# Kernel tuning notes

Hardware: AMD Instinct MI355X
Metric: run time of the kernel (lower is better)

## Reference

```python
import jax, jax.numpy as jnp
import numpy as np

N, E, D0, D1, H = 20000, 640000, 64, 32, 64


def setup_inputs() -> dict:
    key = jax.random.key(0)
    ks = jax.random.split(key, 16)
    s = 0.1
    return {
        'feat0e': jax.random.normal(ks[0], (N, D0), jnp.float32),
        'feat1o': jax.random.normal(ks[1], (N, D1, 3), jnp.float32),
        'edge_attr': jax.random.normal(ks[2], (E, H), jnp.float32),
        'pos': jax.random.normal(ks[3], (N, 3), jnp.float32),
        'edge_index': jax.random.randint(ks[4], (2, E), 0, N, jnp.int64),
        # edge_net: FullyConnectedNet([H]*3 -> [H]) with silu
        'W1': jax.random.normal(ks[5], (H, H), jnp.float32) * s,
        'b1': jnp.zeros((H,), jnp.float32),
        'W2': jax.random.normal(ks[6], (H, H), jnp.float32) * s,
        'b2': jnp.zeros((H,), jnp.float32),
        'W3': jax.random.normal(ks[7], (H, H), jnp.float32) * s,
        'b3': jnp.zeros((H,), jnp.float32),
        # tensor-product path weights (internal weights, not shared)
        'w_ss': jax.random.normal(ks[8], (D0, H, D0), jnp.float32) * s,     # 0e x 0e -> 0e
        'w_vv': jax.random.normal(ks[9], (D1, D0), jnp.float32) * s,        # 1o . 1o -> 0e
        'w_sv': jax.random.normal(ks[10], (D0, D1), jnp.float32) * s,       # 0e x 1o -> 1o
        'w_vs': jax.random.normal(ks[11], (D1, H, D1), jnp.float32) * s,    # 1o x 0e -> 1o
        'w_cross': jax.random.normal(ks[12], (D1, D1), jnp.float32) * s,    # 1o x 1o -> 1o (cross)
        # gate: scalars -> per-vector-channel gates
        'Wg': jax.random.normal(ks[13], (D0, D1), jnp.float32) * s,
        'bg': jnp.zeros((D1,), jnp.float32),
    }


def reference(feat0e, feat1o, edge_attr, pos, edge_index,
              W1, b1, W2, b2, W3, b3,
              w_ss, w_vv, w_sv, w_vs, w_cross, Wg, bg):
    src, dst = edge_index[0], edge_index[1]

    # edge MLP (silu)
    h = jax.nn.silu(edge_attr @ W1 + b1)
    h = jax.nn.silu(h @ W2 + b2)
    edge_scalar = h @ W3 + b3                      # [E, H]

    rel_pos = pos[dst] - pos[src]                  # [E, 3]
    s_src = feat0e[src]                            # [E, D0]
    v_src = feat1o[src]                            # [E, D1, 3]

    # equivariant tensor product per edge
    dot_vv = jnp.sum(v_src * rel_pos[:, None, :], axis=-1)          # [E, D1]
    msg0e = (jnp.einsum('ep,eh,pho->eo', s_src, edge_scalar, w_ss)
             + dot_vv @ w_vv)                                        # [E, D0]
    cross_vv = jnp.cross(v_src, rel_pos[:, None, :])                 # [E, D1, 3]
    msg1o = (jnp.einsum('ep,pc,ex->ecx', s_src, w_sv, rel_pos)
             + jnp.einsum('edx,eh,dhc->ecx', v_src, edge_scalar, w_vs)
             + jnp.einsum('edx,dc->ecx', cross_vv, w_cross))          # [E, D1, 3]

    # scatter_mean over destination nodes
    counts = jax.ops.segment_sum(jnp.ones((E,), msg0e.dtype), dst, num_segments=N)
    denom = jnp.maximum(counts, 1.0)
    aggr0e = jax.ops.segment_sum(msg0e, dst, num_segments=N) / denom[:, None]
    aggr1o = jax.ops.segment_sum(msg1o, dst, num_segments=N) / denom[:, None, None]

    # gate + residual
    out0e = jax.nn.silu(aggr0e) + feat0e                              # [N, D0]
    gates = jax.nn.silu(aggr0e @ Wg + bg)                             # [N, D1]
    out1o = aggr1o * gates[:, :, None] + feat1o                       # [N, D1, 3]

    # concat flattened outputs into one array [N, D0 + 3*D1]
    return jnp.concatenate([out0e, out1o.reshape(N, D1 * 3)], axis=-1)
```

## Files before the change

### kernel.cpp

```cpp
#include <hip/hip_runtime.h>


#define NN 20000
#define EE 640000
#define D0 64
#define D1 32
#define HH 64
#define EPMAX 940032

typedef _Float16 half8 __attribute__((ext_vector_type(8)));
typedef _Float16 half4 __attribute__((ext_vector_type(4)));
typedef float f32x4 __attribute__((ext_vector_type(4)));

__device__ __forceinline__ float silu_f(float x) { return x / (1.0f + __expf(-x)); }
__device__ __forceinline__ _Float16 u2h(unsigned short u) {
    union { unsigned short u; _Float16 h; } c; c.u = u; return c.h;
}
__device__ __forceinline__ unsigned short h2u(_Float16 h) {
    union { unsigned short u; _Float16 h; } c; c.h = h; return c.u;
}
__device__ __forceinline__ half8 pack8(float4 a, float4 b) {
    half8 h;
    h[0]=(_Float16)a.x; h[1]=(_Float16)a.y; h[2]=(_Float16)a.z; h[3]=(_Float16)a.w;
    h[4]=(_Float16)b.x; h[5]=(_Float16)b.y; h[6]=(_Float16)b.z; h[7]=(_Float16)b.w;
    return h;
}

#define OFF_HIST  0ull
#define OFF_RS    81920ull
#define OFF_CUR   163840ull
#define OFF_FLAG  245760ull
#define OFF_SRCA  262144ull
#define OFF_DSTA  2822144ull
#define OFF_PE    5382144ull
#define OFF_WSS   7942144ull
#define OFF_WVS2  8466432ull
#define OFF_WVV   8597504ull
#define OFF_WSV   8601600ull
#define OFF_WX    8605696ull
#define OFF_WMLP  8607744ull
#define OFF_MSG   8632320ull
#define WS_R4_NEED 131512320ull
#define OFF_WSSG  131512320ull
#define OFF_OUTD  132036608ull
#define OFF_PSP   132118528ull
#define OFF_CURS  132200448ull
#define OFF_DSTP  132282368ull
#define OFF_PEP   136042496ull
#define OFF_PDP   139802624ull
#define OFF_G     143562752ull
#define NEED_S(npp) (OFF_G + (unsigned long long)(npp) * 8192ull)

__global__ void detect_idx_kernel(const int* __restrict__ eidx, int* __restrict__ flag) {
    int odd_nz = 0, even_nz = 0;
    for (int k = 0; k < 64; ++k) {
        if (eidx[2 * k + 1] != 0) odd_nz = 1;
        if (eidx[2 * k] != 0) even_nz = 1;
    }
    *flag = (!odd_nz && even_nz) ? 1 : 0;
}

__device__ __forceinline__ void load_sd(const int* eidx, const int* flag, int e,
                                        int& s_, int& d_) {
    if (*flag) { s_ = (int)((const long long*)eidx)[e]; d_ = (int)((const long long*)eidx)[EE + e]; }
    else       { s_ = eidx[e];                          d_ = eidx[EE + e]; }
}

__global__ __launch_bounds__(256) void hist_kernel(
    const int* __restrict__ eidx, const int* __restrict__ flag, int* __restrict__ hist)
{
    const int e = blockIdx.x * 256 + threadIdx.x;
    int s_, d_; load_sd(eidx, flag, e, s_, d_);
    atomicAdd(hist + d_, 1);
}

__global__ __launch_bounds__(256) void hist2_kernel(
    const int* __restrict__ eidx, const int* __restrict__ flag,
    int* __restrict__ hist, int* __restrict__ outd)
{
    const int e = blockIdx.x * 256 + threadIdx.x;
    int s_, d_; load_sd(eidx, flag, e, s_, d_);
    atomicAdd(hist + d_, 1);
    atomicAdd(outd + s_, 1);
}

__global__ __launch_bounds__(1024) void scan_kernel(
    const int* __restrict__ hist, int* __restrict__ rs, int* __restrict__ cur)
{
    __shared__ int part[1024];
    const int t = threadIdx.x;
    const int base = t * 20;
    int loc[20];
    int tot = 0;
#pragma unroll
    for (int k = 0; k < 20; ++k) {
        int n = base + k;
        int h = (n < NN) ? hist[n] : 0;
        loc[k] = tot; tot += h;
    }
    part[t] = tot;
    __syncthreads();
    for (int off = 1; off < 1024; off <<= 1) {
        int v = (t >= off) ? part[t - off] : 0;
        __syncthreads();
        part[t] += v;
        __syncthreads();
    }
    int excl = part[t] - tot;
#pragma unroll
    for (int k = 0; k < 20; ++k) {
        int n = base + k;
        if (n < NN) { rs[n] = excl + loc[k]; cur[n] = excl + loc[k]; }
    }
    if (t == 1023) rs[NN] = part[1023];
}

__global__ __launch_bounds__(1024) void scanP_kernel(
    const int* __restrict__ outd, int* __restrict__ psP, int* __restrict__ curS)
{
    __shared__ int part[1024];
    const int t = threadIdx.x;
    const int base = t * 20;
    int loc[20];
    int tot = 0;
#pragma unroll
    for (int k = 0; k < 20; ++k) {
        int n = base + k;
        int p = (n < NN) ? ((outd[n] + 15) & ~15) : 0;
        loc[k] = tot; tot += p;
    }
    part[t] = tot;
    __syncthreads();
    for (int off = 1; off < 1024; off <<= 1) {
        int v = (t >= off) ? part[t - off] : 0;
        __syncthreads();
        part[t] += v;
        __syncthreads();
    }
    int excl = part[t] - tot;
#pragma unroll
    for (int k = 0; k < 20; ++k) {
        int n = base + k;
        if (n < NN) { psP[n] = excl + loc[k]; curS[n] = excl + loc[k]; }
    }
}

__global__ __launch_bounds__(256) void scat_both_kernel(
    const int* __restrict__ eidx, const int* __restrict__ flag,
    int* __restrict__ curS, int* __restrict__ cur,
    int* __restrict__ dstP, int* __restrict__ peP, int* __restrict__ pdP,
    int* __restrict__ srca, int* __restrict__ dsta, int* __restrict__ pe)
{
    const int e = blockIdx.x * 256 + threadIdx.x;
    int s_, d_; load_sd(eidx, flag, e, s_, d_);
    int posS = atomicAdd(curS + s_, 1);
    int posD = atomicAdd(cur + d_, 1);
    dstP[posS] = d_; peP[posS] = e; pdP[posS] = posD;
    srca[posD] = s_; dsta[posD] = d_; pe[posD] = e;
}

__global__ __launch_bounds__(256) void scatter_r4_kernel(
    const int* __restrict__ eidx, const int* __restrict__ flag,
    int* __restrict__ cur, int* __restrict__ srca, int* __restrict__ dsta,
    int* __restrict__ pe)
{
    const int e = blockIdx.x * 256 + threadIdx.x;
    int s_, d_; load_sd(eidx, flag, e, s_, d_);
    int pos = atomicAdd(cur + d_, 1);
    srca[pos] = s_; dsta[pos] = d_; pe[pos] = e;
}

__global__ __launch_bounds__(256) void prep_kernel(
    const float* __restrict__ wss, const float* __restrict__ wvv,
    const float* __restrict__ wsv, const float* __restrict__ wvs,
    const float* __restrict__ wx,
    const float* __restrict__ W1, const float* __restrict__ W2,
    const float* __restrict__ W3, char* __restrict__ ws, int maxid)
{
    int id = blockIdx.x * 256 + threadIdx.x;
    if (id >= maxid) return;
    int l = id & 63;
    int l4 = l >> 4, l16 = l & 15;
    half8 o;
    _Float16* dst;
    if (id < 32768) {
        int p = id >> 9; int frag = (id >> 6) & 7;
        int kf = frag >> 2, nf = frag & 3;
#pragma unroll
        for (int j = 0; j < 8; j++) {
            int h = kf * 32 + l4 * 8 + j, oo = nf * 16 + l16;
            o[j] = (_Float16)wss[((size_t)p * 64 + h) * 64 + oo];
        }
        dst = (_Float16*)(ws + OFF_WSS) + (size_t)id * 8;
    } else if (id < 40960) {
        int i = id - 32768;
        int f = i >> 6;
        int chunk = f >> 3, kf = (f >> 2) & 1, nfl = f & 3;
#pragma unroll
        for (int j = 0; j < 8; j++) {
            int h = kf * 32 + l4 * 8 + j;
            int col = chunk * 64 + nfl * 16 + l16;
            int d = col >> 5, c = col & 31;
            o[j] = (_Float16)wvs[((size_t)d * 64 + h) * 32 + c];
        }
        dst = (_Float16*)(ws + OFF_WVS2) + (size_t)i * 8;
    } else if (id < 41216) {
        int i = id - 40960; int nf = i >> 6;
#pragma unroll
        for (int j = 0; j < 8; j++) {
            int d = l4 * 8 + j, oo = nf * 16 + l16;
            o[j] = (_Float16)wvv[d * 64 + oo];
        }
        dst = (_Float16*)(ws + OFF_WVV) + (size_t)i * 8;
    } else if (id < 41472) {
        int i = id - 41216; int frag = i >> 6;
        int kf = frag >> 1, nf = frag & 1;
#pragma unroll
        for (int j = 0; j < 8; j++) {
            int p = kf * 32 + l4 * 8 + j, c = nf * 16 + l16;
            o[j] = (_Float16)wsv[p * 32 + c];
        }
        dst = (_Float16*)(ws + OFF_WSV) + (size_t)i * 8;
    } else if (id < 41600) {
        int i = id - 41472; int nf = i >> 6;
#pragma unroll
        for (int j = 0; j < 8; j++) {
            int d = l4 * 8 + j, c = nf * 16 + l16;
            o[j] = (_Float16)wx[d * 32 + c];
        }
        dst = (_Float16*)(ws + OFF_WX) + (size_t)i * 8;
    } else if (id < 43136) {
        int i = id - 41600; int f = i >> 6;
        int layer = f >> 3, kf = (f >> 2) & 1, nf = f & 3;
        const float* W = layer == 0 ? W1 : (layer == 1 ? W2 : W3);
#pragma unroll
        for (int j = 0; j < 8; j++) {
            int r = kf * 32 + l4 * 8 + j, cc = nf * 16 + l16;
            o[j] = (_Float16)W[r * 64 + cc];
        }
        dst = (_Float16*)(ws + OFF_WMLP) + (size_t)i * 8;
    } else {
        int i = id - 43136;
        int f = i >> 6;
        int q = f >> 3, kfp = (f >> 2) & 1, nfp = f & 3;
#pragma unroll
        for (int j = 0; j < 8; j++) {
            int p = kfp * 32 + l4 * 8 + j;
            int cc = q * 64 + nfp * 16 + l16;
            int jc = cc & 7, lc = (cc >> 3) & 63, fi = cc >> 9;
            int kfc = fi >> 2, nfc = fi & 3;
            int h = kfc * 32 + (lc >> 4) * 8 + jc;
            int oo = nfc * 16 + (lc & 15);
            o[j] = (_Float16)wss[((size_t)p * 64 + h) * 64 + oo];
        }
        dst = (_Float16*)(ws + OFF_WSSG) + (size_t)i * 8;
    }
    *(half8*)dst = o;
}

__global__ __launch_bounds__(256, 2) void gG_kernel(
    const float* __restrict__ feat0e, const char* __restrict__ wsp,
    int lo, int hi, _Float16* __restrict__ G)
{
    const int tid = threadIdx.x, w = tid >> 6, lane = tid & 63;
    const int l4 = lane >> 4, l16 = lane & 15;
    const int n0 = lo + blockIdx.x * 64 + w * 16;
    if (n0 >= hi) return;

    half8 af[2];
    {
        int n = n0 + l16; if (n >= NN) n = NN - 1;
        const float* sp = feat0e + (size_t)n * 64 + l4 * 8;
        af[0] = pack8(*(const float4*)sp, *(const float4*)(sp + 4));
        af[1] = pack8(*(const float4*)(sp + 32), *(const float4*)(sp + 36));
    }
    const half8* wg = (const half8*)(wsp + OFF_WSSG);
    for (int q = 0; q < 64; ++q) {
        f32x4 acc[4];
#pragma unroll
        for (int nf = 0; nf < 4; nf++) acc[nf] = (f32x4){0.f,0.f,0.f,0.f};
#pragma unroll
        for (int kf = 0; kf < 2; kf++)
#pragma unroll
            for (int nf = 0; nf < 4; nf++)
                acc[nf] = __builtin_amdgcn_mfma_f32_16x16x32_f16(
                    af[kf], wg[(q * 8 + kf * 4 + nf) * 64 + lane], acc[nf], 0, 0, 0);
#pragma unroll
        for (int nf = 0; nf < 4; nf++)
#pragma unroll
            for (int reg = 0; reg < 4; reg++) {
                int n = n0 + l4 * 4 + reg;
                if (n < hi && n < NN)
                    G[(size_t)(n - lo) * 4096 + q * 64 + nf * 16 + l16] =
                        (_Float16)acc[nf][reg];
            }
    }
}

__device__ __forceinline__ void mlp_wave(
    const float* __restrict__ edge_attr,
    const float* __restrict__ b1, const float* __restrict__ b2,
    const float* __restrict__ b3,
    const char* __restrict__ wsp,
    const int* __restrict__ pel_w,
    unsigned short* __restrict__ xch,
    int lane, half8 esf[4][2])
{
    const int l4 = lane >> 4, l16 = lane & 15;
    const half8* wm = (const half8*)(wsp + OFF_WMLP);

    float bias[3][4];
#pragma unroll
    for (int nf = 0; nf < 4; nf++) {
        bias[0][nf] = b1[nf * 16 + l16];
        bias[1][nf] = b2[nf * 16 + l16];
        bias[2][nf] = b3[nf * 16 + l16];
    }

    half8 af[4][2];
#pragma unroll
    for (int mf = 0; mf < 4; mf++) {
        int e = pel_w[mf * 16 + l16];
        const float* p = edge_attr + (size_t)e * 64 + l4 * 8;
#pragma unroll
        for (int kf = 0; kf < 2; kf++)
            af[mf][kf] = pack8(*(const float4*)(p + kf * 32),
                               *(const float4*)(p + kf * 32 + 4));
    }

#pragma unroll
    for (int layer = 0; layer < 3; ++layer) {
        f32x4 acc[4][4];
#pragma unroll
        for (int mf = 0; mf < 4; mf++)
#pragma unroll
            for (int nf = 0; nf < 4; nf++) acc[mf][nf] = (f32x4){0.f,0.f,0.f,0.f};
#pragma unroll
        for (int kf = 0; kf < 2; kf++)
#pragma unroll
            for (int mf = 0; mf < 4; mf++)
#pragma unroll
                for (int nf = 0; nf < 4; nf++)
                    acc[mf][nf] = __builtin_amdgcn_mfma_f32_16x16x32_f16(
                        af[mf][kf], wm[(layer * 8 + kf * 4 + nf) * 64 + lane],
                        acc[mf][nf], 0, 0, 0);
#pragma unroll
        for (int mf = 0; mf < 4; mf++)
#pragma unroll
            for (int nf = 0; nf < 4; nf++)
#pragma unroll
                for (int reg = 0; reg < 4; reg++) {
                    int row = mf * 16 + l4 * 4 + reg;
                    int col = nf * 16 + l16;
                    float v = acc[mf][nf][reg] + bias[layer][nf];
                    if (layer < 2) v = silu_f(v);
                    xch[row * 64 + (col ^ ((row & 7) << 3))] = h2u((_Float16)v);
                }
        if (layer < 2) {
#pragma unroll
            for (int mf = 0; mf < 4; mf++)
#pragma unroll
                for (int kf = 0; kf < 2; kf++) {
                    int row = mf * 16 + l16;
                    int cs = kf * 32 + l4 * 8;
                    af[mf][kf] = *(const half8*)&xch[row * 64 + (cs ^ ((row & 7) << 3))];
                }
        }
    }
#pragma unroll
    for (int mf = 0; mf < 4; mf++)
#pragma unroll
        for (int kf = 0; kf < 2; kf++) {
            int row = mf * 16 + l16;
            int cs = kf * 32 + l4 * 8;
            esf[mf][kf] = *(const half8*)&xch[row * 64 + (cs ^ ((row & 7) << 3))];
        }
}

__global__ __launch_bounds__(256, 3) void msg0e_node_kernel(
    const float* __restrict__ feat1o,
    const float* __restrict__ edge_attr,
    const float* __restrict__ pos,
    const float* __restrict__ b1, const float* __restrict__ b2,
    const float* __restrict__ b3,
    const char* __restrict__ wsp,
    const _Float16* __restrict__ G,
    int lo, int hi,
    _Float16* __restrict__ msg0)
{
    __shared__ half8 wml[1536];
    __shared__ __align__(16) unsigned short xch[4][1024];

    const int tid = threadIdx.x, w = tid >> 6, lane = tid & 63;
    const int l4 = lane >> 4, l16 = lane & 15;

    {
        const half8* wm = (const half8*)(wsp + OFF_WMLP);
        for (int f = tid; f < 1536; f += 256) wml[f] = wm[f];
    }
    __syncthreads();

    const int n = lo + blockIdx.x * 4 + w;
    if (n >= hi) return;
    const int deg = ((const int*)(wsp + OFF_OUTD))[n];
    if (deg == 0) return;
    const int base = ((const int*)(wsp + OFF_PSP))[n];
    const int* dstP = (const int*)(wsp + OFF_DSTP);
    const int* peP  = (const int*)(wsp + OFF_PEP);
    const int* pdP  = (const int*)(wsp + OFF_PDP);

    const float pn0 = pos[n * 3 + 0], pn1 = pos[n * 3 + 1], pn2 = pos[n * 3 + 2];
    half8 Gr[8];
    {
        const half8* gn = (const half8*)G + (size_t)(n - lo) * 512;
#pragma unroll
        for (int f = 0; f < 8; f++) Gr[f] = gn[f * 64 + lane];
    }
    half8 wvvf[4];
    {
        const half8* wvvp = (const half8*)(wsp + OFF_WVV);
#pragma unroll
        for (int nf = 0; nf < 4; nf++) wvvf[nf] = wvvp[nf * 64 + lane];
    }
    float vx[8], vy[8], vz[8];
#pragma unroll
    for (int j = 0; j < 8; j++) {
        int d = l4 * 8 + j;
        vx[j] = feat1o[(size_t)n * 96 + d * 3 + 0];
        vy[j] = feat1o[(size_t)n * 96 + d * 3 + 1];
        vz[j] = feat1o[(size_t)n * 96 + d * 3 + 2];
    }
    float bias[3][4];
#pragma unroll
    for (int nf = 0; nf < 4; nf++) {
        bias[0][nf] = b1[nf * 16 + l16];
        bias[1][nf] = b2[nf * 16 + l16];
        bias[2][nf] = b3[nf * 16 + l16];
    }

    unsigned short* x = xch[w];
    const int ntile = (deg + 15) >> 4;
    const int sw16 = (l16 & 7) << 3;

    for (int t = 0; t < ntile; ++t) {
        const int r0 = t * 16;
        int rowc = r0 + l16; if (rowc > deg - 1) rowc = deg - 1;
        const int pe = peP[base + rowc];
        const int dd = dstP[base + rowc];
        const float rel0 = pos[dd * 3 + 0] - pn0;
        const float rel1 = pos[dd * 3 + 1] - pn1;
        const float rel2 = pos[dd * 3 + 2] - pn2;

        half8 af[2];
        {
            const float* ap = edge_attr + (size_t)pe * 64 + l4 * 8;
            af[0] = pack8(*(const float4*)ap, *(const float4*)(ap + 4));
            af[1] = pack8(*(const float4*)(ap + 32), *(const float4*)(ap + 36));
        }
#pragma unroll
        for (int layer = 0; layer < 3; ++layer) {
            f32x4 acc[4];
#pragma unroll
            for (int nf = 0; nf < 4; nf++) acc[nf] = (f32x4){0.f,0.f,0.f,0.f};
#pragma unroll
            for (int kf = 0; kf < 2; kf++)
#pragma unroll
                for (int nf = 0; nf < 4; nf++)
                    acc[nf] = __builtin_amdgcn_mfma_f32_16x16x32_f16(
                        af[kf], wml[(layer * 8 + kf * 4 + nf) * 64 + lane],
                        acc[nf], 0, 0, 0);
#pragma unroll
            for (int nf = 0; nf < 4; nf++)
#pragma unroll
                for (int reg = 0; reg < 4; reg++) {
                    int row = l4 * 4 + reg;
                    int col = nf * 16 + l16;
                    float v = acc[nf][reg] + bias[layer][nf];
                    if (layer < 2) v = silu_f(v);
                    x[row * 64 + (col ^ ((row & 7) << 3))] = h2u((_Float16)v);
                }
            if (layer < 2) {
#pragma unroll
                for (int kf = 0; kf < 2; kf++)
                    af[kf] = *(const half8*)&x[l16 * 64 + ((kf * 32 + l4 * 8) ^ sw16)];
            }
        }
        half8 esf[2];
#pragma unroll
        for (int kf = 0; kf < 2; kf++)
            esf[kf] = *(const half8*)&x[l16 * 64 + ((kf * 32 + l4 * 8) ^ sw16)];

        f32x4 acc[4];
#pragma unroll
        for (int nf = 0; nf < 4; nf++) acc[nf] = (f32x4){0.f,0.f,0.f,0.f};
#pragma unroll
        for (int kf = 0; kf < 2; kf++)
#pragma unroll
            for (int nf = 0; nf < 4; nf++)
                acc[nf] = __builtin_amdgcn_mfma_f32_16x16x32_f16(
                    esf[kf], Gr[kf * 4 + nf], acc[nf], 0, 0, 0);
        half8 dvf;
#pragma unroll
        for (int j = 0; j < 8; j++)
            dvf[j] = (_Float16)(vx[j] * rel0 + vy[j] * rel1 + vz[j] * rel2);
#pragma unroll
        for (int nf = 0; nf < 4; nf++)
            acc[nf] = __builtin_amdgcn_mfma_f32_16x16x32_f16(
                dvf, wvvf[nf], acc[nf], 0, 0, 0);

#pragma unroll
        for (int nf = 0; nf < 4; nf++)
#pragma unroll
            for (int reg = 0; reg < 4; reg++) {
                int row = l4 * 4 + reg;
                int col = nf * 16 + l16;
                x[row * 64 + (col ^ ((row & 7) << 3))] = h2u((_Float16)acc[nf][reg]);
            }
#pragma unroll
        for (int i = 0; i < 2; i++) {
            int row16 = i * 8 + (lane >> 3);
            if (r0 + row16 < deg) {
                int rowD = pdP[base + r0 + row16];
                int c8 = lane & 7;
                half8 v = *(const half8*)&x[row16 * 64 + ((c8 * 8) ^ ((row16 & 7) << 3))];
                *(half8*)(msg0 + (size_t)rowD * 64 + c8 * 8) = v;
            }
        }
    }
}

__global__ __launch_bounds__(256, 2) void msg0e_r4_kernel(
    const float* __restrict__ feat0e,
    const float* __restrict__ feat1o,
    const float* __restrict__ edge_attr,
    const float* __restrict__ pos,
    const float* __restrict__ b1, const float* __restrict__ b2,
    const float* __restrict__ b3,
    const char* __restrict__ wsp,
    _Float16* __restrict__ msg0)
{
    __shared__ unsigned short st[4][4096];
    __shared__ unsigned short wf[16384];
    __shared__ float rell[4][64][3];
    __shared__ int   srcl[4][64];
    __shared__ int   pel[4][64];

    const int tid = threadIdx.x, w = tid >> 6, lane = tid & 63;
    const int l4 = lane >> 4, l16 = lane & 15;
    const long i0 = (long)blockIdx.x * 256 + w * 64;

    {
        long p = i0 + lane;
        int s_ = ((const int*)(wsp + OFF_SRCA))[p];
        int d_ = ((const int*)(wsp + OFF_DSTA))[p];
        pel[w][lane] = ((const int*)(wsp + OFF_PE))[p];
        srcl[w][lane] = s_;
        rell[w][lane][0] = pos[d_ * 3 + 0] - pos[s_ * 3 + 0];
        rell[w][lane][1] = pos[d_ * 3 + 1] - pos[s_ * 3 + 1];
        rell[w][lane][2] = pos[d_ * 3 + 2] - pos[s_ * 3 + 2];
    }
    __syncthreads();

    half8 esf[4][2];
    mlp_wave(edge_attr, b1, b2, b3, wsp, pel[w], st[w], lane, esf);
    __syncthreads();

#pragma unroll
    for (int r4 = 0; r4 < 4; r4++) {
        int row = r4 * 16 + (lane >> 2);
        int ch = lane & 3;
        const float* sp = feat0e + (size_t)srcl[w][row] * 64 + ch * 16;
        half8 h0 = pack8(*(const float4*)(sp + 0), *(const float4*)(sp + 4));
        half8 h1 = pack8(*(const float4*)(sp + 8), *(const float4*)(sp + 12));
        int r7 = row & 7;
        *(half8*)&st[w][row * 64 + (((ch * 2) ^ r7) * 8)]     = h0;
        *(half8*)&st[w][row * 64 + (((ch * 2 + 1) ^ r7) * 8)] = h1;
    }
    __syncthreads();

    f32x4 acc[4][4];
#pragma unroll
    for (int mf = 0; mf < 4; mf++)
#pragma unroll
        for (int nf = 0; nf < 4; nf++) acc[mf][nf] = (f32x4){0.f, 0.f, 0.f, 0.f};

    const half8* wss_g = (const half8*)(wsp + OFF_WSS);
    half8* wfh = (half8*)wf;
    for (int pc = 0; pc < 16; ++pc) {
        __syncthreads();
#pragma unroll
        for (int q = 0; q < 8; q++)
            wfh[q * 256 + tid] = wss_g[pc * 2048 + q * 256 + tid];
        __syncthreads();
#pragma unroll
        for (int pl = 0; pl < 4; ++pl) {
            const int p = pc * 4 + pl;
            _Float16 sv[4];
#pragma unroll
            for (int mf = 0; mf < 4; mf++) {
                int row = mf * 16 + l16;
                sv[mf] = u2h(st[w][row * 64 + (((p >> 3) ^ (row & 7)) * 8) + (p & 7)]);
            }
#pragma unroll
            for (int kf = 0; kf < 2; kf++) {
                half8 bf[4];
#pragma unroll
                for (int nf = 0; nf < 4; nf++)
                    bf[nf] = wfh[(pl * 8 + kf * 4 + nf) * 64 + lane];
#pragma unroll
                for (int mf = 0; mf < 4; mf++) {
                    half8 a = esf[mf][kf] * sv[mf];
#pragma unroll
                    for (int nf = 0; nf < 4; nf++)
                        acc[mf][nf] = __builtin_amdgcn_mfma_f32_16x16x32_f16(a, bf[nf], acc[mf][nf], 0, 0, 0);
                }
            }
        }
    }

    half8 dvf[4];
#pragma unroll
    for (int mf = 0; mf < 4; mf++) {
        int row = mf * 16 + l16;
        int se = srcl[w][row];
        float r0 = rell[w][row][0], r1 = rell[w][row][1], r2 = rell[w][row][2];
        const float* vp = feat1o + (size_t)se * 96 + l4 * 24;
        float4 A = *(const float4*)(vp + 0),  B = *(const float4*)(vp + 4);
        float4 C = *(const float4*)(vp + 8),  D = *(const float4*)(vp + 12);
        float4 E = *(const float4*)(vp + 16), F = *(const float4*)(vp + 20);
        dvf[mf][0] = (_Float16)(A.x * r0 + A.y * r1 + A.z * r2);
        dvf[mf][1] = (_Float16)(A.w * r0 + B.x * r1 + B.y * r2);
        dvf[mf][2] = (_Float16)(B.z * r0 + B.w * r1 + C.x * r2);
        dvf[mf][3] = (_Float16)(C.y * r0 + C.z * r1 + C.w * r2);
        dvf[mf][4] = (_Float16)(D.x * r0 + D.y * r1 + D.z * r2);
        dvf[mf][5] = (_Float16)(D.w * r0 + E.x * r1 + E.y * r2);
        dvf[mf][6] = (_Float16)(E.z * r0 + E.w * r1 + F.x * r2);
        dvf[mf][7] = (_Float16)(F.y * r0 + F.z * r1 + F.w * r2);
    }
    const half8* wvvp = (const half8*)(wsp + OFF_WVV);
#pragma unroll
    for (int nf = 0; nf < 4; nf++) {
        half8 bvv = wvvp[nf * 64 + lane];
#pragma unroll
        for (int mf = 0; mf < 4; mf++)
            acc[mf][nf] = __builtin_amdgcn_mfma_f32_16x16x32_f16(dvf[mf], bvv, acc[mf][nf], 0, 0, 0);
    }

#pragma unroll
    for (int mf = 0; mf < 4; mf++)
#pragma unroll
        for (int nf = 0; nf < 4; nf++)
#pragma unroll
            for (int reg = 0; reg < 4; reg++) {
                int row = mf * 16 + l4 * 4 + reg;
                int col = nf * 16 + l16;
                st[w][row * 64 + (col ^ ((row & 7) << 3))] = h2u((_Float16)acc[mf][nf][reg]);
            }
#pragma unroll
    for (int t = 0; t < 8; t++) {
        int row = t * 8 + (lane >> 3);
        int c8 = lane & 7;
        half8 v = *(const half8*)&st[w][row * 64 + ((c8 * 8) ^ ((row & 7) << 3))];
        *(half8*)(msg0 + (size_t)(i0 + row) * 64 + c8 * 8) = v;
    }
}

__global__ __launch_bounds__(256, 2) void msg1o_kernel(
    const float* __restrict__ feat0e,
    const float* __restrict__ feat1o,
    const float* __restrict__ edge_attr,
    const float* __restrict__ pos,
    const float* __restrict__ b1, const float* __restrict__ b2,
    const float* __restrict__ b3,
    const char* __restrict__ wsp,
    _Float16* __restrict__ msg1)
{
    __shared__ unsigned short vt[4][6144];
    __shared__ float rell[4][64][3];
    __shared__ int srcl[4][64];
    __shared__ int pel[4][64];

    const int tid = threadIdx.x, w = tid >> 6, lane = tid & 63;
    const int l4 = lane >> 4, l16 = lane & 15;
    const long i0 = (long)blockIdx.x * 256 + w * 64;

    {
        long p = i0 + lane;
        int s_ = ((const int*)(wsp + OFF_SRCA))[p];
        int d_ = ((const int*)(wsp + OFF_DSTA))[p];
        pel[w][lane] = ((const int*)(wsp + OFF_PE))[p];
        srcl[w][lane] = s_;
        rell[w][lane][0] = pos[d_ * 3 + 0] - pos[s_ * 3 + 0];
        rell[w][lane][1] = pos[d_ * 3 + 1] - pos[s_ * 3 + 1];
        rell[w][lane][2] = pos[d_ * 3 + 2] - pos[s_ * 3 + 2];
    }
    __syncthreads();

    half8 esf[4][2];
    mlp_wave(edge_attr, b1, b2, b3, wsp, pel[w], vt[w], lane, esf);
    __syncthreads();

    {
        const float* vp = feat1o + (size_t)srcl[w][lane] * 96;
#pragma unroll
        for (int q = 0; q < 24; q++) {
            float4 f = *(const float4*)(vp + q * 4);
            vt[w][(q * 4 + 0) * 64 + lane] = h2u((_Float16)f.x);
            vt[w][(q * 4 + 1) * 64 + lane] = h2u((_Float16)f.y);
            vt[w][(q * 4 + 2) * 64 + lane] = h2u((_Float16)f.z);
            vt[w][(q * 4 + 3) * 64 + lane] = h2u((_Float16)f.w);
        }
    }
    __syncthreads();

    const half8* wvs2p = (const half8*)(wsp + OFF_WVS2);
    const half8* wsvp  = (const half8*)(wsp + OFF_WSV);
    const half8* wxp   = (const half8*)(wsp + OFF_WX);

    f32x4 acc1[4][3][2];
#pragma unroll
    for (int g = 0; g < 4; g++)
#pragma unroll
        for (int x = 0; x < 3; x++)
#pragma unroll
            for (int ch = 0; ch < 2; ch++) acc1[g][x][ch] = (f32x4){0.f,0.f,0.f,0.f};

#pragma unroll 2
    for (int ck = 0; ck < 16; ++ck) {
        half8 bf[2][4];
#pragma unroll
        for (int kf = 0; kf < 2; kf++)
#pragma unroll
            for (int nfl = 0; nfl < 4; nfl++)
                bf[kf][nfl] = wvs2p[(ck * 8 + kf * 4 + nfl) * 64 + lane];
#pragma unroll
        for (int g = 0; g < 4; g++) {
            f32x4 tacc[4];
#pragma unroll
            for (int nfl = 0; nfl < 4; nfl++) tacc[nfl] = (f32x4){0.f,0.f,0.f,0.f};
#pragma unroll
            for (int kf = 0; kf < 2; kf++)
#pragma unroll
                for (int nfl = 0; nfl < 4; nfl++)
                    tacc[nfl] = __builtin_amdgcn_mfma_f32_16x16x32_f16(
                        esf[g][kf], bf[kf][nfl], tacc[nfl], 0, 0, 0);
#pragma unroll
            for (int dl = 0; dl < 2; dl++) {
                int d = ck * 2 + dl;
#pragma unroll
                for (int x = 0; x < 3; x++) {
                    half4 hv = *(const half4*)&vt[w][(d * 3 + x) * 64 + g * 16 + l4 * 4];
                    f32x4 vf = __builtin_convertvector(hv, f32x4);
                    acc1[g][x][0] += vf * tacc[dl * 2 + 0];
                    acc1[g][x][1] += vf * tacc[dl * 2 + 1];
                }
            }
        }
    }

    {
        half8 bsv[2][2];
#pragma unroll
        for (int kf = 0; kf < 2; kf++)
#pragma unroll
            for (int nf = 0; nf < 2; nf++)
                bsv[kf][nf] = wsvp[(size_t)(kf * 2 + nf) * 64 + lane];
#pragma unroll
        for (int g = 0; g < 4; g++) {
            int erow = g * 16 + l16;
            const float* sp = feat0e + (size_t)srcl[w][erow] * 64 + l4 * 8;
            half8 sf[2];
#pragma unroll
            for (int kf = 0; kf < 2; kf++)
                sf[kf] = pack8(*(const float4*)(sp + kf * 32),
                               *(const float4*)(sp + kf * 32 + 4));
#pragma unroll
            for (int x = 0; x < 3; x++) {
                _Float16 rl = (_Float16)rell[w][erow][x];
#pragma unroll
                for (int kf = 0; kf < 2; kf++) {
                    half8 a = sf[kf] * rl;
#pragma unroll
                    for (int nf = 0; nf < 2; nf++)
                        acc1[g][x][nf] = __builtin_amdgcn_mfma_f32_16x16x32_f16(
                            a, bsv[kf][nf], acc1[g][x][nf], 0, 0, 0);
                }
            }
        }
    }

    {
        half8 bx[2];
        bx[0] = wxp[lane];
        bx[1] = wxp[64 + lane];
#pragma unroll
        for (int g = 0; g < 4; g++) {
            f32x4 cx[3][2];
#pragma unroll
            for (int xp = 0; xp < 3; xp++) {
                half8 av;
#pragma unroll
                for (int j = 0; j < 8; j++)
                    av[j] = u2h(vt[w][((l4 * 8 + j) * 3 + xp) * 64 + g * 16 + l16]);
#pragma unroll
                for (int nf = 0; nf < 2; nf++)
                    cx[xp][nf] = __builtin_amdgcn_mfma_f32_16x16x32_f16(
                        av, bx[nf], (f32x4){0.f,0.f,0.f,0.f}, 0, 0, 0);
            }
            f32x4 r[3];
#pragma unroll
            for (int x = 0; x < 3; x++)
#pragma unroll
                for (int reg = 0; reg < 4; reg++)
                    r[x][reg] = rell[w][g * 16 + l4 * 4 + reg][x];
#pragma unroll
            for (int x = 0; x < 3; x++) {
                const int x1 = (x + 1) % 3, x2 = (x + 2) % 3;
#pragma unroll
                for (int ch = 0; ch < 2; ch++)
                    acc1[g][x][ch] += r[x2] * cx[x1][ch] - r[x1] * cx[x2][ch];
            }
        }
    }

    __syncthreads();
#pragma unroll
    for (int g = 0; g < 4; g++)
#pragma unroll
        for (int reg = 0; reg < 4; reg++) {
            int row = g * 16 + l4 * 4 + reg;
            int sw = (row & 3) << 3;
#pragma unroll
            for (int x = 0; x < 3; x++)
#pragma unroll
                for (int ch = 0; ch < 2; ch++) {
                    int c32 = ch * 16 + l16;
                    vt[w][row * 96 + x * 32 + (c32 ^ sw)] = h2u((_Float16)acc1[g][x][ch][reg]);
                }
        }
#pragma unroll
    for (int tt = 0; tt < 12; tt++) {
        int x = tt >> 2, rem = (tt & 3) * 8;
        int col = x * 32 + (rem ^ ((lane & 3) << 3));
        half8 v = *(const half8*)&vt[w][lane * 96 + col];
        *(half8*)(msg1 + (size_t)(i0 + lane) * 96 + tt * 8) = v;
    }
}

__global__ __launch_bounds__(256) void gather0_kernel(
    const float* __restrict__ feat0e,
    const float* __restrict__ Wg, const float* __restrict__ bg,
    const char* __restrict__ wsp, const _Float16* __restrict__ msg0,
    float* __restrict__ out)
{
    __shared__ float Wgl[2048];
    __shared__ float ag[4][64];
    const int tid = threadIdx.x, w = tid >> 6, lane = tid & 63;
    for (int t = tid; t < 2048; t += 256) Wgl[t] = Wg[t];

    const int n = blockIdx.x * 4 + w;
    const int* rs = (const int*)(wsp + OFF_RS);
    const int i0 = rs[n], i1 = rs[n + 1];
    const int r8 = lane >> 3, c8 = lane & 7;

    float a[8];
#pragma unroll
    for (int j = 0; j < 8; j++) a[j] = 0.f;
    for (int i = i0 + r8; i < i1; i += 8) {
        half8 m = *(const half8*)(msg0 + (size_t)i * 64 + c8 * 8);
#pragma unroll
        for (int j = 0; j < 8; j++) a[j] += (float)m[j];
    }
#pragma unroll
    for (int s = 8; s < 64; s <<= 1)
#pragma unroll
        for (int j = 0; j < 8; j++) a[j] += __shfl_xor(a[j], s);
    if (r8 == 0)
#pragma unroll
        for (int j = 0; j < 8; j++) ag[w][c8 * 8 + j] = a[j];
    __syncthreads();

    const float inv = 1.0f / fmaxf((float)(i1 - i0), 1.0f);
    float av = ag[w][lane] * inv;
    out[(size_t)n * 160 + lane] = silu_f(av) + feat0e[(size_t)n * 64 + lane];

    if (lane < 32) {
        float gs = bg[lane];
#pragma unroll
        for (int p = 0; p < 64; ++p) gs = fmaf(ag[w][p] * inv, Wgl[p * 32 + lane], gs);
        out[(size_t)n * 160 + 64 + lane] = silu_f(gs);
    }
}

__global__ __launch_bounds__(256) void gather1_kernel(
    const float* __restrict__ feat1o,
    const char* __restrict__ wsp, const _Float16* __restrict__ msg1,
    float* __restrict__ out)
{
    __shared__ float ag1[4][96];
    __shared__ float gl[4][32];
    const int tid = threadIdx.x, w = tid >> 6, lane = tid & 63;
    const int n = blockIdx.x * 4 + w;
    const int* rs = (const int*)(wsp + OFF_RS);
    const int i0 = rs[n], i1 = rs[n + 1];

    if (lane < 32) gl[w][lane] = out[(size_t)n * 160 + 64 + lane];

    const int r4 = lane >> 4, c12 = lane & 15;
    float a[8];
#pragma unroll
    for (int j = 0; j < 8; j++) a[j] = 0.f;
    if (c12 < 12)
        for (int i = i0 + r4; i < i1; i += 4) {
            half8 m = *(const half8*)(msg1 + (size_t)i * 96 + c12 * 8);
#pragma unroll
            for (int j = 0; j < 8; j++) a[j] += (float)m[j];
        }
#pragma unroll
    for (int s = 16; s < 64; s <<= 1)
#pragma unroll
        for (int j = 0; j < 8; j++) a[j] += __shfl_xor(a[j], s);
    if (r4 == 0 && c12 < 12)
#pragma unroll
        for (int j = 0; j < 8; j++) ag1[w][c12 * 8 + j] = a[j];
    __syncthreads();

    const float inv = 1.0f / fmaxf((float)(i1 - i0), 1.0f);
#pragma unroll
    for (int t = 0; t < 2; t++) {
        int idx = t * 64 + lane;
        if (idx < 96) {
            int c = idx / 3, x = idx - 3 * c;
            float v = ag1[w][x * 32 + c] * inv * gl[w][c] + feat1o[(size_t)n * 96 + idx];
            out[(size_t)n * 160 + 64 + idx] = v;
        }
    }
}

extern "C" void kernel_launch(void* const* d_in, const int* in_sizes, int n_in,
                              void* d_out, int out_size, void* d_ws, size_t ws_size,
                              hipStream_t stream) {
    const float* feat0e    = (const float*)d_in[0];
    const float* feat1o    = (const float*)d_in[1];
    const float* edge_attr = (const float*)d_in[2];
    const float* pos       = (const float*)d_in[3];
    const int*   eidx      = (const int*)d_in[4];
    const float* W1 = (const float*)d_in[5];
    const float* b1 = (const float*)d_in[6];
    const float* W2 = (const float*)d_in[7];
    const float* b2 = (const float*)d_in[8];
    const float* W3 = (const float*)d_in[9];
    const float* b3 = (const float*)d_in[10];
    const float* wss    = (const float*)d_in[11];
    const float* wvv    = (const float*)d_in[12];
    const float* wsv    = (const float*)d_in[13];
    const float* wvs    = (const float*)d_in[14];
    const float* wcross = (const float*)d_in[15];
    const float* Wg = (const float*)d_in[16];
    const float* bg = (const float*)d_in[17];

    float* out = (float*)d_out;
    char*  ws  = (char*)d_ws;
    int* hist = (int*)(ws + OFF_HIST);
    int* rs   = (int*)(ws + OFF_RS);
    int* cur  = (int*)(ws + OFF_CUR);
    int* flag = (int*)(ws + OFF_FLAG);
    int* srca = (int*)(ws + OFF_SRCA);
    int* dsta = (int*)(ws + OFF_DSTA);
    int* pe   = (int*)(ws + OFF_PE);
    _Float16* msg = (_Float16*)(ws + OFF_MSG);

    detect_idx_kernel<<<1, 1, 0, stream>>>(eidx, flag);
    hipMemsetAsync(ws + OFF_HIST, 0, NN * sizeof(int), stream);

    int S = 0;
    if (ws_size >= NEED_S(20000)) S = 1;
    else if (ws_size >= NEED_S(10000)) S = 2;
    else if (ws_size >= NEED_S(5000))  S = 4;
    else if (ws_size >= NEED_S(2500))  S = 8;

    if (S > 0) {
        int* outd = (int*)(ws + OFF_OUTD);
        int* psP  = (int*)(ws + OFF_PSP);
        int* curS = (int*)(ws + OFF_CURS);
        int* dstP = (int*)(ws + OFF_DSTP);
        int* peP  = (int*)(ws + OFF_PEP);
        int* pdP  = (int*)(ws + OFF_PDP);
        _Float16* G = (_Float16*)(ws + OFF_G);

        hipMemsetAsync(ws + OFF_OUTD, 0, NN * sizeof(int), stream);

        hist2_kernel<<<EE / 256, 256, 0, stream>>>(eidx, flag, hist, outd);
        scan_kernel<<<1, 1024, 0, stream>>>(hist, rs, cur);
        scanP_kernel<<<1, 1024, 0, stream>>>(outd, psP, curS);
        scat_both_kernel<<<EE / 256, 256, 0, stream>>>(
            eidx, flag, curS, cur, dstP, peP, pdP, srca, dsta, pe);
        prep_kernel<<<(75904 + 255) / 256, 256, 0, stream>>>(
            wss, wvv, wsv, wvs, wcross, W1, W2, W3, ws, 75904);

        const int npp = (NN + S - 1) / S;
        for (int s = 0; s < S; ++s) {
            int lo = s * npp;
            int hi = lo + npp; if (hi > NN) hi = NN;
            gG_kernel<<<(hi - lo + 63) / 64, 256, 0, stream>>>(
                feat0e, (const char*)ws, lo, hi, G);
            msg0e_node_kernel<<<(hi - lo + 3) / 4, 256, 0, stream>>>(
                feat1o, edge_attr, pos, b1, b2, b3, (const char*)ws, G, lo, hi, msg);
        }
        gather0_kernel<<<NN / 4, 256, 0, stream>>>(
            feat0e, Wg, bg, (const char*)ws, msg, out);
        msg1o_kernel<<<EE / 256, 256, 0, stream>>>(
            feat0e, feat1o, edge_attr, pos, b1, b2, b3, (const char*)ws, msg);
        gather1_kernel<<<NN / 4, 256, 0, stream>>>(
            feat1o, (const char*)ws, msg, out);
    } else {
        hist_kernel<<<EE / 256, 256, 0, stream>>>(eidx, flag, hist);
        scan_kernel<<<1, 1024, 0, stream>>>(hist, rs, cur);
        scatter_r4_kernel<<<EE / 256, 256, 0, stream>>>(eidx, flag, cur, srca, dsta, pe);
        prep_kernel<<<(43136 + 255) / 256, 256, 0, stream>>>(
            wss, wvv, wsv, wvs, wcross, W1, W2, W3, ws, 43136);
        msg0e_r4_kernel<<<EE / 256, 256, 0, stream>>>(
            feat0e, feat1o, edge_attr, pos, b1, b2, b3, (const char*)ws, msg);
        gather0_kernel<<<NN / 4, 256, 0, stream>>>(
            feat0e, Wg, bg, (const char*)ws, msg, out);
        msg1o_kernel<<<EE / 256, 256, 0, stream>>>(
            feat0e, feat1o, edge_attr, pos, b1, b2, b3, (const char*)ws, msg);
        gather1_kernel<<<NN / 4, 256, 0, stream>>>(
            feat1o, (const char*)ws, msg, out);
    }
}
```

Baseline: 849.5 us.

## Precompute per-source-node tensor-product projections and fuse msg0e/msg1o into one node pass

Moves the per-edge tensor-product weight contractions to per-source-node precomputation. gG2 and gH build G/H tables from feat0e and feat1o against w_ss, w_vs, w_vv, w_sv and w_cross. A separate es_kernel computes the edge MLP once into a buffer, and a single msg01_node_kernel walks edges grouped by source to produce both msg0e and msg1o. This replaces the separate per-edge msg1o kernel and removes the fallback path. The aim is to remove redundant per-edge MFMA work and a second pass over edge_attr, at the cost of a much larger workspace footprint (GH per node plus ES/MSG buffers). If the workspace is too small the function now returns without computing anything.

```diff
diff --git a/kernel.cpp b/kernel.cpp
--- a/kernel.cpp
+++ b/kernel.cpp
@@ -3,13 +3,9 @@
 
 #define NN 20000
 #define EE 640000
-#define D0 64
-#define D1 32
-#define HH 64
 #define EPMAX 940032
 
 typedef _Float16 half8 __attribute__((ext_vector_type(8)));
-typedef _Float16 half4 __attribute__((ext_vector_type(4)));
 typedef float f32x4 __attribute__((ext_vector_type(4)));
 
 __device__ __forceinline__ float silu_f(float x) { return x / (1.0f + __expf(-x)); }
@@ -30,26 +26,24 @@
 #define OFF_RS    81920ull
 #define OFF_CUR   163840ull
 #define OFF_FLAG  245760ull
-#define OFF_SRCA  262144ull
-#define OFF_DSTA  2822144ull
-#define OFF_PE    5382144ull
-#define OFF_WSS   7942144ull
-#define OFF_WVS2  8466432ull
-#define OFF_WVV   8597504ull
-#define OFF_WSV   8601600ull
-#define OFF_WX    8605696ull
-#define OFF_WMLP  8607744ull
-#define OFF_MSG   8632320ull
-#define WS_R4_NEED 131512320ull
-#define OFF_WSSG  131512320ull
-#define OFF_OUTD  132036608ull
-#define OFF_PSP   132118528ull
-#define OFF_CURS  132200448ull
-#define OFF_DSTP  132282368ull
-#define OFF_PEP   136042496ull
-#define OFF_PDP   139802624ull
-#define OFF_G     143562752ull
-#define NEED_S(npp) (OFF_G + (unsigned long long)(npp) * 8192ull)
+#define F_OUTD    262144ull
+#define F_PSP     360448ull
+#define F_CURS    458752ull
+#define F_POSOF   557056ull
+#define F_AUX     3117056ull
+#define F_DSTP    23597056ull
+#define F_PDP     27357184ull
+#define F_WMLP    31117312ull
+#define F_WSV     31141888ull
+#define F_WX2     31145984ull
+#define F_WVV     31148032ull
+#define F_WSSG    31152128ull
+#define F_WVS3    31676416ull
+#define F_ES      31807488ull
+#define F_MSG0    152131584ull
+#define F_MSG1    234051584ull
+#define F_GH      356931584ull
+#define NEED_F(npp) (F_GH + (unsigned long long)(npp) * 20480ull)
 
 __global__ void detect_idx_kernel(const int* __restrict__ eidx, int* __restrict__ flag) {
     int odd_nz = 0, even_nz = 0;
@@ -64,14 +58,6 @@
                                         int& s_, int& d_) {
     if (*flag) { s_ = (int)((const long long*)eidx)[e]; d_ = (int)((const long long*)eidx)[EE + e]; }
     else       { s_ = eidx[e];                          d_ = eidx[EE + e]; }
-}
-
-__global__ __launch_bounds__(256) void hist_kernel(
-    const int* __restrict__ eidx, const int* __restrict__ flag, int* __restrict__ hist)
-{
-    const int e = blockIdx.x * 256 + threadIdx.x;
-    int s_, d_; load_sd(eidx, flag, e, s_, d_);
-    atomicAdd(hist + d_, 1);
 }
 
 __global__ __launch_bounds__(256) void hist2_kernel(
@@ -145,102 +131,33 @@
     }
 }
 
-__global__ __launch_bounds__(256) void scat_both_kernel(
+__global__ __launch_bounds__(256) void scat_src_kernel(
     const int* __restrict__ eidx, const int* __restrict__ flag,
     int* __restrict__ curS, int* __restrict__ cur,
-    int* __restrict__ dstP, int* __restrict__ peP, int* __restrict__ pdP,
-    int* __restrict__ srca, int* __restrict__ dsta, int* __restrict__ pe)
+    int* __restrict__ dstP, int* __restrict__ pdP, int* __restrict__ posof)
 {
     const int e = blockIdx.x * 256 + threadIdx.x;
     int s_, d_; load_sd(eidx, flag, e, s_, d_);
     int posS = atomicAdd(curS + s_, 1);
     int posD = atomicAdd(cur + d_, 1);
-    dstP[posS] = d_; peP[posS] = e; pdP[posS] = posD;
-    srca[posD] = s_; dsta[posD] = d_; pe[posD] = e;
-}
-
-__global__ __launch_bounds__(256) void scatter_r4_kernel(
-    const int* __restrict__ eidx, const int* __restrict__ flag,
-    int* __restrict__ cur, int* __restrict__ srca, int* __restrict__ dsta,
-    int* __restrict__ pe)
-{
-    const int e = blockIdx.x * 256 + threadIdx.x;
-    int s_, d_; load_sd(eidx, flag, e, s_, d_);
-    int pos = atomicAdd(cur + d_, 1);
-    srca[pos] = s_; dsta[pos] = d_; pe[pos] = e;
-}
-
-__global__ __launch_bounds__(256) void prep_kernel(
+    dstP[posS] = d_; pdP[posS] = posD; posof[e] = posS;
+}
+
+__global__ __launch_bounds__(256) void prep2_kernel(
     const float* __restrict__ wss, const float* __restrict__ wvv,
     const float* __restrict__ wsv, const float* __restrict__ wvs,
     const float* __restrict__ wx,
     const float* __restrict__ W1, const float* __restrict__ W2,
-    const float* __restrict__ W3, char* __restrict__ ws, int maxid)
+    const float* __restrict__ W3, char* __restrict__ ws)
 {
     int id = blockIdx.x * 256 + threadIdx.x;
-    if (id >= maxid) return;
+    if (id >= 43136) return;
     int l = id & 63;
     int l4 = l >> 4, l16 = l & 15;
     half8 o;
     _Float16* dst;
     if (id < 32768) {
-        int p = id >> 9; int frag = (id >> 6) & 7;
-        int kf = frag >> 2, nf = frag & 3;
-#pragma unroll
-        for (int j = 0; j < 8; j++) {
-            int h = kf * 32 + l4 * 8 + j, oo = nf * 16 + l16;
-            o[j] = (_Float16)wss[((size_t)p * 64 + h) * 64 + oo];
-        }
-        dst = (_Float16*)(ws + OFF_WSS) + (size_t)id * 8;
-    } else if (id < 40960) {
-        int i = id - 32768;
-        int f = i >> 6;
-        int chunk = f >> 3, kf = (f >> 2) & 1, nfl = f & 3;
-#pragma unroll
-        for (int j = 0; j < 8; j++) {
-            int h = kf * 32 + l4 * 8 + j;
-            int col = chunk * 64 + nfl * 16 + l16;
-            int d = col >> 5, c = col & 31;
-            o[j] = (_Float16)wvs[((size_t)d * 64 + h) * 32 + c];
-        }
-        dst = (_Float16*)(ws + OFF_WVS2) + (size_t)i * 8;
-    } else if (id < 41216) {
-        int i = id - 40960; int nf = i >> 6;
-#pragma unroll
-        for (int j = 0; j < 8; j++) {
-            int d = l4 * 8 + j, oo = nf * 16 + l16;
-            o[j] = (_Float16)wvv[d * 64 + oo];
-        }
-        dst = (_Float16*)(ws + OFF_WVV) + (size_t)i * 8;
-    } else if (id < 41472) {
-        int i = id - 41216; int frag = i >> 6;
-        int kf = frag >> 1, nf = frag & 1;
-#pragma unroll
-        for (int j = 0; j < 8; j++) {
-            int p = kf * 32 + l4 * 8 + j, c = nf * 16 + l16;
-            o[j] = (_Float16)wsv[p * 32 + c];
-        }
-        dst = (_Float16*)(ws + OFF_WSV) + (size_t)i * 8;
-    } else if (id < 41600) {
-        int i = id - 41472; int nf = i >> 6;
-#pragma unroll
-        for (int j = 0; j < 8; j++) {
-            int d = l4 * 8 + j, c = nf * 16 + l16;
-            o[j] = (_Float16)wx[d * 32 + c];
-        }
-        dst = (_Float16*)(ws + OFF_WX) + (size_t)i * 8;
-    } else if (id < 43136) {
-        int i = id - 41600; int f = i >> 6;
-        int layer = f >> 3, kf = (f >> 2) & 1, nf = f & 3;
-        const float* W = layer == 0 ? W1 : (layer == 1 ? W2 : W3);
-#pragma unroll
-        for (int j = 0; j < 8; j++) {
-            int r = kf * 32 + l4 * 8 + j, cc = nf * 16 + l16;
-            o[j] = (_Float16)W[r * 64 + cc];
-        }
-        dst = (_Float16*)(ws + OFF_WMLP) + (size_t)i * 8;
-    } else {
-        int i = id - 43136;
+        int i = id;
         int f = i >> 6;
         int q = f >> 3, kfp = (f >> 2) & 1, nfp = f & 3;
 #pragma unroll
@@ -253,14 +170,51 @@
             int oo = nfc * 16 + (lc & 15);
             o[j] = (_Float16)wss[((size_t)p * 64 + h) * 64 + oo];
         }
-        dst = (_Float16*)(ws + OFF_WSSG) + (size_t)i * 8;
+        dst = (_Float16*)(ws + F_WSSG) + (size_t)i * 8;
+    } else if (id < 40960) {
+        int i = id - 32768;
+        int f = i >> 6;
+        int col = f * 16 + l16;
+#pragma unroll
+        for (int j = 0; j < 8; j++) {
+            int d = l4 * 8 + j;
+            o[j] = (_Float16)wvs[((size_t)d * 64 + (col & 63)) * 32 + (col >> 6)];
+        }
+        dst = (_Float16*)(ws + F_WVS3) + (size_t)i * 8;
+    } else if (id < 42496) {
+        int i = id - 40960; int f = i >> 6;
+        int layer = f >> 3, kf = (f >> 2) & 1, nf = f & 3;
+        const float* W = layer == 0 ? W1 : (layer == 1 ? W2 : W3);
+#pragma unroll
+        for (int j = 0; j < 8; j++)
+            o[j] = (_Float16)W[(kf * 32 + l4 * 8 + j) * 64 + nf * 16 + l16];
+        dst = (_Float16*)(ws + F_WMLP) + (size_t)i * 8;
+    } else if (id < 42752) {
+        int i = id - 42496; int nf = i >> 6;
+#pragma unroll
+        for (int j = 0; j < 8; j++)
+            o[j] = (_Float16)wvv[(l4 * 8 + j) * 64 + nf * 16 + l16];
+        dst = (_Float16*)(ws + F_WVV) + (size_t)i * 8;
+    } else if (id < 43008) {
+        int i = id - 42752; int frag = i >> 6;
+        int kf = frag >> 1, nf = frag & 1;
+#pragma unroll
+        for (int j = 0; j < 8; j++)
+            o[j] = (_Float16)wsv[(kf * 32 + l4 * 8 + j) * 32 + nf * 16 + l16];
+        dst = (_Float16*)(ws + F_WSV) + (size_t)i * 8;
+    } else {
+        int i = id - 43008; int nf = i >> 6;
+#pragma unroll
+        for (int j = 0; j < 8; j++)
+            o[j] = (_Float16)wx[(l4 * 8 + j) * 32 + nf * 16 + l16];
+        dst = (_Float16*)(ws + F_WX2) + (size_t)i * 8;
     }
     *(half8*)dst = o;
 }
 
-__global__ __launch_bounds__(256, 2) void gG_kernel(
+__global__ __launch_bounds__(256, 2) void gG2_kernel(
     const float* __restrict__ feat0e, const char* __restrict__ wsp,
-    int lo, int hi, _Float16* __restrict__ G)
+    int lo, int hi, _Float16* __restrict__ GH, _Float16* __restrict__ aux)
 {
     const int tid = threadIdx.x, w = tid >> 6, lane = tid & 63;
     const int l4 = lane >> 4, l16 = lane & 15;
@@ -274,7 +228,7 @@
         af[0] = pack8(*(const float4*)sp, *(const float4*)(sp + 4));
         af[1] = pack8(*(const float4*)(sp + 32), *(const float4*)(sp + 36));
     }
-    const half8* wg = (const half8*)(wsp + OFF_WSSG);
+    const half8* wg = (const half8*)(wsp + F_WSSG);
     for (int q = 0; q < 64; ++q) {
         f32x4 acc[4];
 #pragma unroll
@@ -291,23 +245,113 @@
             for (int reg = 0; reg < 4; reg++) {
                 int n = n0 + l4 * 4 + reg;
                 if (n < hi && n < NN)
-                    G[(size_t)(n - lo) * 4096 + q * 64 + nf * 16 + l16] =
+                    GH[(size_t)(n - lo) * 10240 + q * 64 + nf * 16 + l16] =
                         (_Float16)acc[nf][reg];
             }
     }
-}
-
-__device__ __forceinline__ void mlp_wave(
+    {
+        const half8* wsvp = (const half8*)(wsp + F_WSV);
+        f32x4 accg[2];
+#pragma unroll
+        for (int nf = 0; nf < 2; nf++) accg[nf] = (f32x4){0.f,0.f,0.f,0.f};
+#pragma unroll
+        for (int kf = 0; kf < 2; kf++)
+#pragma unroll
+            for (int nf = 0; nf < 2; nf++)
+                accg[nf] = __builtin_amdgcn_mfma_f32_16x16x32_f16(
+                    af[kf], wsvp[(kf * 2 + nf) * 64 + lane], accg[nf], 0, 0, 0);
+#pragma unroll
+        for (int nf = 0; nf < 2; nf++)
+#pragma unroll
+            for (int reg = 0; reg < 4; reg++) {
+                int n = n0 + l4 * 4 + reg;
+                if (n < hi && n < NN)
+                    aux[(size_t)n * 512 + nf * 16 + l16] = (_Float16)accg[nf][reg];
+            }
+    }
+}
+
+__global__ __launch_bounds__(256, 2) void gH_kernel(
+    const float* __restrict__ feat1o, const char* __restrict__ wsp,
+    int lo, int hi, _Float16* __restrict__ GH, _Float16* __restrict__ aux)
+{
+    const int tid = threadIdx.x, w = tid >> 6, lane = tid & 63;
+    const int l4 = lane >> 4, l16 = lane & 15;
+    const int n0 = lo + blockIdx.x * 64 + w * 16;
+    if (n0 >= hi) return;
+
+    const half8* wvs3 = (const half8*)(wsp + F_WVS3);
+    const half8* wvvp = (const half8*)(wsp + F_WVV);
+    const half8* wx2  = (const half8*)(wsp + F_WX2);
+
+#pragma unroll 1
+    for (int x = 0; x < 3; ++x) {
+        half8 av;
+        {
+            int nn = n0 + l16; if (nn >= NN) nn = NN - 1;
+#pragma unroll
+            for (int j = 0; j < 8; j++)
+                av[j] = (_Float16)feat1o[(size_t)nn * 96 + (l4 * 8 + j) * 3 + x];
+        }
+#pragma unroll 4
+        for (int f = 0; f < 128; ++f) {
+            f32x4 acc = __builtin_amdgcn_mfma_f32_16x16x32_f16(
+                av, wvs3[f * 64 + lane], (f32x4){0.f,0.f,0.f,0.f}, 0, 0, 0);
+#pragma unroll
+            for (int reg = 0; reg < 4; reg++) {
+                int n = n0 + l4 * 4 + reg;
+                if (n < hi && n < NN)
+                    GH[(size_t)(n - lo) * 10240 + 4096 + x * 2048 + f * 16 + l16] =
+                        (_Float16)acc[reg];
+            }
+        }
+#pragma unroll
+        for (int nf = 0; nf < 4; ++nf) {
+            f32x4 acc = __builtin_amdgcn_mfma_f32_16x16x32_f16(
+                av, wvvp[nf * 64 + lane], (f32x4){0.f,0.f,0.f,0.f}, 0, 0, 0);
+#pragma unroll
+            for (int reg = 0; reg < 4; reg++) {
+                int n = n0 + l4 * 4 + reg;
+                if (n < hi && n < NN)
+                    aux[(size_t)n * 512 + 128 + x * 64 + nf * 16 + l16] =
+                        (_Float16)acc[reg];
+            }
+        }
+#pragma unroll
+        for (int nf = 0; nf < 2; ++nf) {
+            f32x4 acc = __builtin_amdgcn_mfma_f32_16x16x32_f16(
+                av, wx2[nf * 64 + lane], (f32x4){0.f,0.f,0.f,0.f}, 0, 0, 0);
+#pragma unroll
+            for (int reg = 0; reg < 4; reg++) {
+                int n = n0 + l4 * 4 + reg;
+                if (n < hi && n < NN)
+                    aux[(size_t)n * 512 + 32 + x * 32 + nf * 16 + l16] =
+                        (_Float16)acc[reg];
+            }
+        }
+    }
+}
+
+__global__ __launch_bounds__(256, 2) void es_kernel(
     const float* __restrict__ edge_attr,
     const float* __restrict__ b1, const float* __restrict__ b2,
     const float* __restrict__ b3,
-    const char* __restrict__ wsp,
-    const int* __restrict__ pel_w,
-    unsigned short* __restrict__ xch,
-    int lane, half8 esf[4][2])
-{
+    const char* __restrict__ wsp, const int* __restrict__ posof,
+    _Float16* __restrict__ es)
+{
+    __shared__ half8 wml[1536];
+    __shared__ __align__(16) unsigned short xch[4][1024];
+
+    const int tid = threadIdx.x, w = tid >> 6, lane = tid & 63;
     const int l4 = lane >> 4, l16 = lane & 15;
-    const half8* wm = (const half8*)(wsp + OFF_WMLP);
+
+    {
+        const half8* wm = (const half8*)(wsp + F_WMLP);
+        for (int f = tid; f < 1536; f += 256) wml[f] = wm[f];
+    }
+    __syncthreads();
+
+    const int e0 = blockIdx.x * 64 + w * 16;
 
     float bias[3][4];
 #pragma unroll
@@ -317,533 +361,203 @@
         bias[2][nf] = b3[nf * 16 + l16];
     }
 
-    half8 af[4][2];
-#pragma unroll
-    for (int mf = 0; mf < 4; mf++) {
-        int e = pel_w[mf * 16 + l16];
-        const float* p = edge_attr + (size_t)e * 64 + l4 * 8;
+    half8 af[2];
+    {
+        const float* ap = edge_attr + (size_t)(e0 + l16) * 64 + l4 * 8;
+        af[0] = pack8(*(const float4*)ap, *(const float4*)(ap + 4));
+        af[1] = pack8(*(const float4*)(ap + 32), *(const float4*)(ap + 36));
+    }
+
+    unsigned short* x = xch[w];
+    const int sw16 = (l16 & 7) << 3;
+
+#pragma unroll
+    for (int layer = 0; layer < 3; ++layer) {
+        f32x4 acc[4];
+#pragma unroll
+        for (int nf = 0; nf < 4; nf++) acc[nf] = (f32x4){0.f,0.f,0.f,0.f};
 #pragma unroll
         for (int kf = 0; kf < 2; kf++)
-            af[mf][kf] = pack8(*(const float4*)(p + kf * 32),
-                               *(const float4*)(p + kf * 32 + 4));
-    }
-
-#pragma unroll
-    for (int layer = 0; layer < 3; ++layer) {
-        f32x4 acc[4][4];
-#pragma unroll
-        for (int mf = 0; mf < 4; mf++)
-#pragma unroll
-            for (int nf = 0; nf < 4; nf++) acc[mf][nf] = (f32x4){0.f,0.f,0.f,0.f};
-#pragma unroll
-        for (int kf = 0; kf < 2; kf++)
-#pragma unroll
-            for (int mf = 0; mf < 4; mf++)
-#pragma unroll
-                for (int nf = 0; nf < 4; nf++)
-                    acc[mf][nf] = __builtin_amdgcn_mfma_f32_16x16x32_f16(
-                        af[mf][kf], wm[(layer * 8 + kf * 4 + nf) * 64 + lane],
-                        acc[mf][nf], 0, 0, 0);
-#pragma unroll
-        for (int mf = 0; mf < 4; mf++)
 #pragma unroll
             for (int nf = 0; nf < 4; nf++)
-#pragma unroll
-                for (int reg = 0; reg < 4; reg++) {
-                    int row = mf * 16 + l4 * 4 + reg;
-                    int col = nf * 16 + l16;
-                    float v = acc[mf][nf][reg] + bias[layer][nf];
-                    if (layer < 2) v = silu_f(v);
-                    xch[row * 64 + (col ^ ((row & 7) << 3))] = h2u((_Float16)v);
-                }
+                acc[nf] = __builtin_amdgcn_mfma_f32_16x16x32_f16(
+                    af[kf], wml[(layer * 8 + kf * 4 + nf) * 64 + lane],
+                    acc[nf], 0, 0, 0);
+#pragma unroll
+        for (int nf = 0; nf < 4; nf++)
+#pragma unroll
+            for (int reg = 0; reg < 4; reg++) {
+                int row = l4 * 4 + reg;
+                int col = nf * 16 + l16;
+                float v = acc[nf][reg] + bias[layer][nf];
+                if (layer < 2) v = silu_f(v);
+                x[row * 64 + (col ^ ((row & 7) << 3))] = h2u((_Float16)v);
+            }
         if (layer < 2) {
 #pragma unroll
-            for (int mf = 0; mf < 4; mf++)
-#pragma unroll
-                for (int kf = 0; kf < 2; kf++) {
-                    int row = mf * 16 + l16;
-                    int cs = kf * 32 + l4 * 8;
-                    af[mf][kf] = *(const half8*)&xch[row * 64 + (cs ^ ((row & 7) << 3))];
-                }
-        }
-    }
-#pragma unroll
-    for (int mf = 0; mf < 4; mf++)
-#pragma unroll
-        for (int kf = 0; kf < 2; kf++) {
-            int row = mf * 16 + l16;
-            int cs = kf * 32 + l4 * 8;
-            esf[mf][kf] = *(const half8*)&xch[row * 64 + (cs ^ ((row & 7) << 3))];
-        }
-}
-
-__global__ __launch_bounds__(256, 3) void msg0e_node_kernel(
-    const float* __restrict__ feat1o,
-    const float* __restrict__ edge_attr,
+            for (int kf = 0; kf < 2; kf++)
+                af[kf] = *(const half8*)&x[l16 * 64 + ((kf * 32 + l4 * 8) ^ sw16)];
+        }
+    }
+#pragma unroll
+    for (int i = 0; i < 2; i++) {
+        int row16 = i * 8 + (lane >> 3);
+        int ps = posof[e0 + row16];
+        int c8 = lane & 7;
+        half8 v = *(const half8*)&x[row16 * 64 + ((c8 * 8) ^ ((row16 & 7) << 3))];
+        *(half8*)(es + (size_t)ps * 64 + c8 * 8) = v;
+    }
+}
+
+__global__ __launch_bounds__(256, 3) void msg01_node_kernel(
     const float* __restrict__ pos,
-    const float* __restrict__ b1, const float* __restrict__ b2,
-    const float* __restrict__ b3,
     const char* __restrict__ wsp,
-    const _Float16* __restrict__ G,
+    const _Float16* __restrict__ GH,
+    const _Float16* __restrict__ es,
     int lo, int hi,
-    _Float16* __restrict__ msg0)
-{
-    __shared__ half8 wml[1536];
-    __shared__ __align__(16) unsigned short xch[4][1024];
+    _Float16* __restrict__ msg0, _Float16* __restrict__ msg1)
+{
+    __shared__ __align__(16) unsigned short xch[4][16 * 104];
+    __shared__ float relb[4][16][4];
+    __shared__ unsigned short auxl[4][320];
 
     const int tid = threadIdx.x, w = tid >> 6, lane = tid & 63;
     const int l4 = lane >> 4, l16 = lane & 15;
 
-    {
-        const half8* wm = (const half8*)(wsp + OFF_WMLP);
-        for (int f = tid; f < 1536; f += 256) wml[f] = wm[f];
-    }
-    __syncthreads();
-
     const int n = lo + blockIdx.x * 4 + w;
     if (n >= hi) return;
-    const int deg = ((const int*)(wsp + OFF_OUTD))[n];
+    const int deg = ((const int*)(wsp + F_OUTD))[n];
     if (deg == 0) return;
-    const int base = ((const int*)(wsp + OFF_PSP))[n];
-    const int* dstP = (const int*)(wsp + OFF_DSTP);
-    const int* peP  = (const int*)(wsp + OFF_PEP);
-    const int* pdP  = (const int*)(wsp + OFF_PDP);
+    const int base = ((const int*)(wsp + F_PSP))[n];
+    const int* dstP = (const int*)(wsp + F_DSTP);
+    const int* pdP  = (const int*)(wsp + F_PDP);
 
     const float pn0 = pos[n * 3 + 0], pn1 = pos[n * 3 + 1], pn2 = pos[n * 3 + 2];
+
+    const size_t kbase = (size_t)(n - lo) * 10240;
     half8 Gr[8];
     {
-        const half8* gn = (const half8*)G + (size_t)(n - lo) * 512;
+        const half8* gn = (const half8*)(GH + kbase);
 #pragma unroll
         for (int f = 0; f < 8; f++) Gr[f] = gn[f * 64 + lane];
     }
-    half8 wvvf[4];
+    half8 Hf[2][6];
     {
-        const half8* wvvp = (const half8*)(wsp + OFF_WVV);
-#pragma unroll
-        for (int nf = 0; nf < 4; nf++) wvvf[nf] = wvvp[nf * 64 + lane];
-    }
-    float vx[8], vy[8], vz[8];
-#pragma unroll
-    for (int j = 0; j < 8; j++) {
-        int d = l4 * 8 + j;
-        vx[j] = feat1o[(size_t)n * 96 + d * 3 + 0];
-        vy[j] = feat1o[(size_t)n * 96 + d * 3 + 1];
-        vz[j] = feat1o[(size_t)n * 96 + d * 3 + 2];
-    }
-    float bias[3][4];
-#pragma unroll
-    for (int nf = 0; nf < 4; nf++) {
-        bias[0][nf] = b1[nf * 16 + l16];
-        bias[1][nf] = b2[nf * 16 + l16];
-        bias[2][nf] = b3[nf * 16 + l16];
+        const _Float16* Hg = GH + kbase + 4096;
+#pragma unroll
+        for (int x = 0; x < 3; x++)
+#pragma unroll
+            for (int nfc = 0; nfc < 2; nfc++)
+#pragma unroll
+                for (int kf = 0; kf < 2; kf++)
+                    Hf[kf][x * 2 + nfc] = *(const half8*)(
+                        Hg + x * 2048 + (nfc * 16 + l16) * 64 + kf * 32 + l4 * 8);
+    }
+    {
+        const _Float16* ag = (const _Float16*)(wsp + F_AUX) + (size_t)n * 512;
+        for (int i = lane; i < 320; i += 64) auxl[w][i] = h2u(ag[i]);
     }
 
     unsigned short* x = xch[w];
     const int ntile = (deg + 15) >> 4;
-    const int sw16 = (l16 & 7) << 3;
 
     for (int t = 0; t < ntile; ++t) {
         const int r0 = t * 16;
         int rowc = r0 + l16; if (rowc > deg - 1) rowc = deg - 1;
-        const int pe = peP[base + rowc];
         const int dd = dstP[base + rowc];
         const float rel0 = pos[dd * 3 + 0] - pn0;
         const float rel1 = pos[dd * 3 + 1] - pn1;
         const float rel2 = pos[dd * 3 + 2] - pn2;
-
-        half8 af[2];
+        if (l4 == 0) {
+            relb[w][l16][0] = rel0; relb[w][l16][1] = rel1; relb[w][l16][2] = rel2;
+        }
+
+        half8 esf[2];
         {
-            const float* ap = edge_attr + (size_t)pe * 64 + l4 * 8;
-            af[0] = pack8(*(const float4*)ap, *(const float4*)(ap + 4));
-            af[1] = pack8(*(const float4*)(ap + 32), *(const float4*)(ap + 36));
-        }
-#pragma unroll
-        for (int layer = 0; layer < 3; ++layer) {
-            f32x4 acc[4];
-#pragma unroll
-            for (int nf = 0; nf < 4; nf++) acc[nf] = (f32x4){0.f,0.f,0.f,0.f};
+            const _Float16* ep = es + (size_t)(base + rowc) * 64;
+            esf[0] = *(const half8*)(ep + l4 * 8);
+            esf[1] = *(const half8*)(ep + 32 + l4 * 8);
+        }
+
+        {
+            f32x4 acc0[4];
+#pragma unroll
+            for (int nf = 0; nf < 4; nf++) acc0[nf] = (f32x4){0.f,0.f,0.f,0.f};
 #pragma unroll
             for (int kf = 0; kf < 2; kf++)
 #pragma unroll
                 for (int nf = 0; nf < 4; nf++)
-                    acc[nf] = __builtin_amdgcn_mfma_f32_16x16x32_f16(
-                        af[kf], wml[(layer * 8 + kf * 4 + nf) * 64 + lane],
-                        acc[nf], 0, 0, 0);
-#pragma unroll
-            for (int nf = 0; nf < 4; nf++)
+                    acc0[nf] = __builtin_amdgcn_mfma_f32_16x16x32_f16(
+                        esf[kf], Gr[kf * 4 + nf], acc0[nf], 0, 0, 0);
+#pragma unroll
+            for (int nf = 0; nf < 4; nf++) {
+                float vw0 = (float)u2h(auxl[w][128 + 0 * 64 + nf * 16 + l16]);
+                float vw1 = (float)u2h(auxl[w][128 + 1 * 64 + nf * 16 + l16]);
+                float vw2 = (float)u2h(auxl[w][128 + 2 * 64 + nf * 16 + l16]);
 #pragma unroll
                 for (int reg = 0; reg < 4; reg++) {
                     int row = l4 * 4 + reg;
+                    float v = acc0[nf][reg]
+                            + relb[w][row][0] * vw0
+                            + relb[w][row][1] * vw1
+                            + relb[w][row][2] * vw2;
                     int col = nf * 16 + l16;
-                    float v = acc[nf][reg] + bias[layer][nf];
-                    if (layer < 2) v = silu_f(v);
-                    x[row * 64 + (col ^ ((row & 7) << 3))] = h2u((_Float16)v);
+                    x[row * 104 + (col ^ ((row & 7) << 3))] = h2u((_Float16)v);
                 }
-            if (layer < 2) {
-#pragma unroll
-                for (int kf = 0; kf < 2; kf++)
-                    af[kf] = *(const half8*)&x[l16 * 64 + ((kf * 32 + l4 * 8) ^ sw16)];
-            }
-        }
-        half8 esf[2];
-#pragma unroll
-        for (int kf = 0; kf < 2; kf++)
-            esf[kf] = *(const half8*)&x[l16 * 64 + ((kf * 32 + l4 * 8) ^ sw16)];
-
-        f32x4 acc[4];
-#pragma unroll
-        for (int nf = 0; nf < 4; nf++) acc[nf] = (f32x4){0.f,0.f,0.f,0.f};
-#pragma unroll
-        for (int kf = 0; kf < 2; kf++)
-#pragma unroll
-            for (int nf = 0; nf < 4; nf++)
-                acc[nf] = __builtin_amdgcn_mfma_f32_16x16x32_f16(
-                    esf[kf], Gr[kf * 4 + nf], acc[nf], 0, 0, 0);
-        half8 dvf;
-#pragma unroll
-        for (int j = 0; j < 8; j++)
-            dvf[j] = (_Float16)(vx[j] * rel0 + vy[j] * rel1 + vz[j] * rel2);
-#pragma unroll
-        for (int nf = 0; nf < 4; nf++)
-            acc[nf] = __builtin_amdgcn_mfma_f32_16x16x32_f16(
-                dvf, wvvf[nf], acc[nf], 0, 0, 0);
-
-#pragma unroll
-        for (int nf = 0; nf < 4; nf++)
-#pragma unroll
-            for (int reg = 0; reg < 4; reg++) {
-                int row = l4 * 4 + reg;
-                int col = nf * 16 + l16;
-                x[row * 64 + (col ^ ((row & 7) << 3))] = h2u((_Float16)acc[nf][reg]);
-            }
-#pragma unroll
-        for (int i = 0; i < 2; i++) {
-            int row16 = i * 8 + (lane >> 3);
-            if (r0 + row16 < deg) {
-                int rowD = pdP[base + r0 + row16];
-                int c8 = lane & 7;
-                half8 v = *(const half8*)&x[row16 * 64 + ((c8 * 8) ^ ((row16 & 7) << 3))];
-                *(half8*)(msg0 + (size_t)rowD * 64 + c8 * 8) = v;
-            }
-        }
-    }
-}
-
-__global__ __launch_bounds__(256, 2) void msg0e_r4_kernel(
-    const float* __restrict__ feat0e,
-    const float* __restrict__ feat1o,
-    const float* __restrict__ edge_attr,
-    const float* __restrict__ pos,
-    const float* __restrict__ b1, const float* __restrict__ b2,
-    const float* __restrict__ b3,
-    const char* __restrict__ wsp,
-    _Float16* __restrict__ msg0)
-{
-    __shared__ unsigned short st[4][4096];
-    __shared__ unsigned short wf[16384];
-    __shared__ float rell[4][64][3];
-    __shared__ int   srcl[4][64];
-    __shared__ int   pel[4][64];
-
-    const int tid = threadIdx.x, w = tid >> 6, lane = tid & 63;
-    const int l4 = lane >> 4, l16 = lane & 15;
-    const long i0 = (long)blockIdx.x * 256 + w * 64;
-
-    {
-        long p = i0 + lane;
-        int s_ = ((const int*)(wsp + OFF_SRCA))[p];
-        int d_ = ((const int*)(wsp + OFF_DSTA))[p];
-        pel[w][lane] = ((const int*)(wsp + OFF_PE))[p];
-        srcl[w][lane] = s_;
-        rell[w][lane][0] = pos[d_ * 3 + 0] - pos[s_ * 3 + 0];
-        rell[w][lane][1] = pos[d_ * 3 + 1] - pos[s_ * 3 + 1];
-        rell[w][lane][2] = pos[d_ * 3 + 2] - pos[s_ * 3 + 2];
-    }
-    __syncthreads();
-
-    half8 esf[4][2];
-    mlp_wave(edge_attr, b1, b2, b3, wsp, pel[w], st[w], lane, esf);
-    __syncthreads();
-
-#pragma unroll
-    for (int r4 = 0; r4 < 4; r4++) {
-        int row = r4 * 16 + (lane >> 2);
-        int ch = lane & 3;
-        const float* sp = feat0e + (size_t)srcl[w][row] * 64 + ch * 16;
-        half8 h0 = pack8(*(const float4*)(sp + 0), *(const float4*)(sp + 4));
-        half8 h1 = pack8(*(const float4*)(sp + 8), *(const float4*)(sp + 12));
-        int r7 = row & 7;
-        *(half8*)&st[w][row * 64 + (((ch * 2) ^ r7) * 8)]     = h0;
-        *(half8*)&st[w][row * 64 + (((ch * 2 + 1) ^ r7) * 8)] = h1;
-    }
-    __syncthreads();
-
-    f32x4 acc[4][4];
-#pragma unroll
-    for (int mf = 0; mf < 4; mf++)
-#pragma unroll
-        for (int nf = 0; nf < 4; nf++) acc[mf][nf] = (f32x4){0.f, 0.f, 0.f, 0.f};
-
-    const half8* wss_g = (const half8*)(wsp + OFF_WSS);
-    half8* wfh = (half8*)wf;
-    for (int pc = 0; pc < 16; ++pc) {
-        __syncthreads();
-#pragma unroll
-        for (int q = 0; q < 8; q++)
-            wfh[q * 256 + tid] = wss_g[pc * 2048 + q * 256 + tid];
-        __syncthreads();
-#pragma unroll
-        for (int pl = 0; pl < 4; ++pl) {
-            const int p = pc * 4 + pl;
-            _Float16 sv[4];
-#pragma unroll
-            for (int mf = 0; mf < 4; mf++) {
-                int row = mf * 16 + l16;
-                sv[mf] = u2h(st[w][row * 64 + (((p >> 3) ^ (row & 7)) * 8) + (p & 7)]);
-            }
-#pragma unroll
-            for (int kf = 0; kf < 2; kf++) {
-                half8 bf[4];
-#pragma unroll
-                for (int nf = 0; nf < 4; nf++)
-                    bf[nf] = wfh[(pl * 8 + kf * 4 + nf) * 64 + lane];
-#pragma unroll
-                for (int mf = 0; mf < 4; mf++) {
-                    half8 a = esf[mf][kf] * sv[mf];
-#pragma unroll
-                    for (int nf = 0; nf < 4; nf++)
-                        acc[mf][nf] = __builtin_amdgcn_mfma_f32_16x16x32_f16(a, bf[nf], acc[mf][nf], 0, 0, 0);
+            }
+#pragma unroll
+            for (int i = 0; i < 2; i++) {
+                int row16 = i * 8 + (lane >> 3);
+                if (r0 + row16 < deg) {
+                    int rowD = pdP[base + r0 + row16];
+                    int c8 = lane & 7;
+                    half8 v = *(const half8*)&x[row16 * 104 + ((c8 * 8) ^ ((row16 & 7) << 3))];
+                    *(half8*)(msg0 + (size_t)rowD * 64 + c8 * 8) = v;
                 }
             }
         }
-    }
-
-    half8 dvf[4];
-#pragma unroll
-    for (int mf = 0; mf < 4; mf++) {
-        int row = mf * 16 + l16;
-        int se = srcl[w][row];
-        float r0 = rell[w][row][0], r1 = rell[w][row][1], r2 = rell[w][row][2];
-        const float* vp = feat1o + (size_t)se * 96 + l4 * 24;
-        float4 A = *(const float4*)(vp + 0),  B = *(const float4*)(vp + 4);
-        float4 C = *(const float4*)(vp + 8),  D = *(const float4*)(vp + 12);
-        float4 E = *(const float4*)(vp + 16), F = *(const float4*)(vp + 20);
-        dvf[mf][0] = (_Float16)(A.x * r0 + A.y * r1 + A.z * r2);
-        dvf[mf][1] = (_Float16)(A.w * r0 + B.x * r1 + B.y * r2);
-        dvf[mf][2] = (_Float16)(B.z * r0 + B.w * r1 + C.x * r2);
-        dvf[mf][3] = (_Float16)(C.y * r0 + C.z * r1 + C.w * r2);
-        dvf[mf][4] = (_Float16)(D.x * r0 + D.y * r1 + D.z * r2);
-        dvf[mf][5] = (_Float16)(D.w * r0 + E.x * r1 + E.y * r2);
-        dvf[mf][6] = (_Float16)(E.z * r0 + E.w * r1 + F.x * r2);
-        dvf[mf][7] = (_Float16)(F.y * r0 + F.z * r1 + F.w * r2);
-    }
-    const half8* wvvp = (const half8*)(wsp + OFF_WVV);
-#pragma unroll
-    for (int nf = 0; nf < 4; nf++) {
-        half8 bvv = wvvp[nf * 64 + lane];
-#pragma unroll
-        for (int mf = 0; mf < 4; mf++)
-            acc[mf][nf] = __builtin_amdgcn_mfma_f32_16x16x32_f16(dvf[mf], bvv, acc[mf][nf], 0, 0, 0);
-    }
-
-#pragma unroll
-    for (int mf = 0; mf < 4; mf++)
-#pragma unroll
-        for (int nf = 0; nf < 4; nf++)
-#pragma unroll
-            for (int reg = 0; reg < 4; reg++) {
-                int row = mf * 16 + l4 * 4 + reg;
-                int col = nf * 16 + l16;
-                st[w][row * 64 + (col ^ ((row & 7) << 3))] = h2u((_Float16)acc[mf][nf][reg]);
-            }
-#pragma unroll
-    for (int t = 0; t < 8; t++) {
-        int row = t * 8 + (lane >> 3);
-        int c8 = lane & 7;
-        half8 v = *(const half8*)&st[w][row * 64 + ((c8 * 8) ^ ((row & 7) << 3))];
-        *(half8*)(msg0 + (size_t)(i0 + row) * 64 + c8 * 8) = v;
-    }
-}
-
-__global__ __launch_bounds__(256, 2) void msg1o_kernel(
-    const float* __restrict__ feat0e,
-    const float* __restrict__ feat1o,
-    const float* __restrict__ edge_attr,
-    const float* __restrict__ pos,
-    const float* __restrict__ b1, const float* __restrict__ b2,
-    const float* __restrict__ b3,
-    const char* __restrict__ wsp,
-    _Float16* __restrict__ msg1)
-{
-    __shared__ unsigned short vt[4][6144];
-    __shared__ float rell[4][64][3];
-    __shared__ int srcl[4][64];
-    __shared__ int pel[4][64];
-
-    const int tid = threadIdx.x, w = tid >> 6, lane = tid & 63;
-    const int l4 = lane >> 4, l16 = lane & 15;
-    const long i0 = (long)blockIdx.x * 256 + w * 64;
-
-    {
-        long p = i0 + lane;
-        int s_ = ((const int*)(wsp + OFF_SRCA))[p];
-        int d_ = ((const int*)(wsp + OFF_DSTA))[p];
-        pel[w][lane] = ((const int*)(wsp + OFF_PE))[p];
-        srcl[w][lane] = s_;
-        rell[w][lane][0] = pos[d_ * 3 + 0] - pos[s_ * 3 + 0];
-        rell[w][lane][1] = pos[d_ * 3 + 1] - pos[s_ * 3 + 1];
-        rell[w][lane][2] = pos[d_ * 3 + 2] - pos[s_ * 3 + 2];
-    }
-    __syncthreads();
-
-    half8 esf[4][2];
-    mlp_wave(edge_attr, b1, b2, b3, wsp, pel[w], vt[w], lane, esf);
-    __syncthreads();
-
-    {
-        const float* vp = feat1o + (size_t)srcl[w][lane] * 96;
-#pragma unroll
-        for (int q = 0; q < 24; q++) {
-            float4 f = *(const float4*)(vp + q * 4);
-            vt[w][(q * 4 + 0) * 64 + lane] = h2u((_Float16)f.x);
-            vt[w][(q * 4 + 1) * 64 + lane] = h2u((_Float16)f.y);
-            vt[w][(q * 4 + 2) * 64 + lane] = h2u((_Float16)f.z);
-            vt[w][(q * 4 + 3) * 64 + lane] = h2u((_Float16)f.w);
-        }
-    }
-    __syncthreads();
-
-    const half8* wvs2p = (const half8*)(wsp + OFF_WVS2);
-    const half8* wsvp  = (const half8*)(wsp + OFF_WSV);
-    const half8* wxp   = (const half8*)(wsp + OFF_WX);
-
-    f32x4 acc1[4][3][2];
-#pragma unroll
-    for (int g = 0; g < 4; g++)
-#pragma unroll
-        for (int x = 0; x < 3; x++)
-#pragma unroll
-            for (int ch = 0; ch < 2; ch++) acc1[g][x][ch] = (f32x4){0.f,0.f,0.f,0.f};
-
-#pragma unroll 2
-    for (int ck = 0; ck < 16; ++ck) {
-        half8 bf[2][4];
-#pragma unroll
-        for (int kf = 0; kf < 2; kf++)
-#pragma unroll
-            for (int nfl = 0; nfl < 4; nfl++)
-                bf[kf][nfl] = wvs2p[(ck * 8 + kf * 4 + nfl) * 64 + lane];
-#pragma unroll
-        for (int g = 0; g < 4; g++) {
-            f32x4 tacc[4];
-#pragma unroll
-            for (int nfl = 0; nfl < 4; nfl++) tacc[nfl] = (f32x4){0.f,0.f,0.f,0.f};
+
+        {
+            f32x4 acc1[6];
+#pragma unroll
+            for (int nf = 0; nf < 6; nf++) acc1[nf] = (f32x4){0.f,0.f,0.f,0.f};
 #pragma unroll
             for (int kf = 0; kf < 2; kf++)
 #pragma unroll
-                for (int nfl = 0; nfl < 4; nfl++)
-                    tacc[nfl] = __builtin_amdgcn_mfma_f32_16x16x32_f16(
-                        esf[g][kf], bf[kf][nfl], tacc[nfl], 0, 0, 0);
-#pragma unroll
-            for (int dl = 0; dl < 2; dl++) {
-                int d = ck * 2 + dl;
-#pragma unroll
-                for (int x = 0; x < 3; x++) {
-                    half4 hv = *(const half4*)&vt[w][(d * 3 + x) * 64 + g * 16 + l4 * 4];
-                    f32x4 vf = __builtin_convertvector(hv, f32x4);
-                    acc1[g][x][0] += vf * tacc[dl * 2 + 0];
-                    acc1[g][x][1] += vf * tacc[dl * 2 + 1];
+                for (int nf = 0; nf < 6; nf++)
+                    acc1[nf] = __builtin_amdgcn_mfma_f32_16x16x32_f16(
+                        esf[kf], Hf[kf][nf], acc1[nf], 0, 0, 0);
+#pragma unroll
+            for (int nf = 0; nf < 6; nf++) {
+                const int xx = nf >> 1;
+                const int x1 = (xx + 1) % 3, x2 = (xx + 2) % 3;
+                const int c = (nf & 1) * 16 + l16;
+                const float gv  = (float)u2h(auxl[w][c]);
+                const float cw1 = (float)u2h(auxl[w][32 + x1 * 32 + c]);
+                const float cw2 = (float)u2h(auxl[w][32 + x2 * 32 + c]);
+#pragma unroll
+                for (int reg = 0; reg < 4; reg++) {
+                    int row = l4 * 4 + reg;
+                    float val = acc1[nf][reg]
+                              + gv * relb[w][row][xx]
+                              + relb[w][row][x2] * cw1
+                              - relb[w][row][x1] * cw2;
+                    int col = nf * 16 + l16;
+                    x[row * 104 + (col ^ ((row & 3) << 3))] = h2u((_Float16)val);
                 }
             }
-        }
-    }
-
-    {
-        half8 bsv[2][2];
-#pragma unroll
-        for (int kf = 0; kf < 2; kf++)
-#pragma unroll
-            for (int nf = 0; nf < 2; nf++)
-                bsv[kf][nf] = wsvp[(size_t)(kf * 2 + nf) * 64 + lane];
-#pragma unroll
-        for (int g = 0; g < 4; g++) {
-            int erow = g * 16 + l16;
-            const float* sp = feat0e + (size_t)srcl[w][erow] * 64 + l4 * 8;
-            half8 sf[2];
-#pragma unroll
-            for (int kf = 0; kf < 2; kf++)
-                sf[kf] = pack8(*(const float4*)(sp + kf * 32),
-                               *(const float4*)(sp + kf * 32 + 4));
-#pragma unroll
-            for (int x = 0; x < 3; x++) {
-                _Float16 rl = (_Float16)rell[w][erow][x];
-#pragma unroll
-                for (int kf = 0; kf < 2; kf++) {
-                    half8 a = sf[kf] * rl;
-#pragma unroll
-                    for (int nf = 0; nf < 2; nf++)
-                        acc1[g][x][nf] = __builtin_amdgcn_mfma_f32_16x16x32_f16(
-                            a, bsv[kf][nf], acc1[g][x][nf], 0, 0, 0);
+            const int rowS = lane >> 2;
+            if (r0 + rowS < deg) {
+                int rowD = pdP[base + r0 + rowS];
+                const int swr = (rowS & 3) << 3;
+#pragma unroll
+                for (int t3 = 0; t3 < 3; t3++) {
+                    int co = ((lane & 3) + 4 * t3) * 8;
+                    half8 v = *(const half8*)&x[rowS * 104 + (co ^ swr)];
+                    *(half8*)(msg1 + (size_t)rowD * 96 + co) = v;
                 }
             }
         }
-    }
-
-    {
-        half8 bx[2];
-        bx[0] = wxp[lane];
-        bx[1] = wxp[64 + lane];
-#pragma unroll
-        for (int g = 0; g < 4; g++) {
-            f32x4 cx[3][2];
-#pragma unroll
-            for (int xp = 0; xp < 3; xp++) {
-                half8 av;
-#pragma unroll
-                for (int j = 0; j < 8; j++)
-                    av[j] = u2h(vt[w][((l4 * 8 + j) * 3 + xp) * 64 + g * 16 + l16]);
-#pragma unroll
-                for (int nf = 0; nf < 2; nf++)
-                    cx[xp][nf] = __builtin_amdgcn_mfma_f32_16x16x32_f16(
-                        av, bx[nf], (f32x4){0.f,0.f,0.f,0.f}, 0, 0, 0);
-            }
-            f32x4 r[3];
-#pragma unroll
-            for (int x = 0; x < 3; x++)
-#pragma unroll
-                for (int reg = 0; reg < 4; reg++)
-                    r[x][reg] = rell[w][g * 16 + l4 * 4 + reg][x];
-#pragma unroll
-            for (int x = 0; x < 3; x++) {
-                const int x1 = (x + 1) % 3, x2 = (x + 2) % 3;
-#pragma unroll
-                for (int ch = 0; ch < 2; ch++)
-                    acc1[g][x][ch] += r[x2] * cx[x1][ch] - r[x1] * cx[x2][ch];
-            }
-        }
-    }
-
-    __syncthreads();
-#pragma unroll
-    for (int g = 0; g < 4; g++)
-#pragma unroll
-        for (int reg = 0; reg < 4; reg++) {
-            int row = g * 16 + l4 * 4 + reg;
-            int sw = (row & 3) << 3;
-#pragma unroll
-            for (int x = 0; x < 3; x++)
-#pragma unroll
-                for (int ch = 0; ch < 2; ch++) {
-                    int c32 = ch * 16 + l16;
-                    vt[w][row * 96 + x * 32 + (c32 ^ sw)] = h2u((_Float16)acc1[g][x][ch][reg]);
-                }
-        }
-#pragma unroll
-    for (int tt = 0; tt < 12; tt++) {
-        int x = tt >> 2, rem = (tt & 3) * 8;
-        int col = x * 32 + (rem ^ ((lane & 3) << 3));
-        half8 v = *(const half8*)&vt[w][lane * 96 + col];
-        *(half8*)(msg1 + (size_t)(i0 + lane) * 96 + tt * 8) = v;
     }
 }
 
@@ -930,8 +644,8 @@
     for (int t = 0; t < 2; t++) {
         int idx = t * 64 + lane;
         if (idx < 96) {
-            int c = idx / 3, x = idx - 3 * c;
-            float v = ag1[w][x * 32 + c] * inv * gl[w][c] + feat1o[(size_t)n * 96 + idx];
+            int c = idx / 3, xx = idx - 3 * c;
+            float v = ag1[w][xx * 32 + c] * inv * gl[w][c] + feat1o[(size_t)n * 96 + idx];
             out[(size_t)n * 160 + 64 + idx] = v;
         }
     }
@@ -965,67 +679,52 @@
     int* rs   = (int*)(ws + OFF_RS);
     int* cur  = (int*)(ws + OFF_CUR);
     int* flag = (int*)(ws + OFF_FLAG);
-    int* srca = (int*)(ws + OFF_SRCA);
-    int* dsta = (int*)(ws + OFF_DSTA);
-    int* pe   = (int*)(ws + OFF_PE);
-    _Float16* msg = (_Float16*)(ws + OFF_MSG);
+    int* outd = (int*)(ws + F_OUTD);
+    int* psP  = (int*)(ws + F_PSP);
+    int* curS = (int*)(ws + F_CURS);
+    int* posof= (int*)(ws + F_POSOF);
+    int* dstP = (int*)(ws + F_DSTP);
+    int* pdP  = (int*)(ws + F_PDP);
+    _Float16* aux   = (_Float16*)(ws + F_AUX);
+    _Float16* esb   = (_Float16*)(ws + F_ES);
+    _Float16* msg0F = (_Float16*)(ws + F_MSG0);
+    _Float16* msg1F = (_Float16*)(ws + F_MSG1);
+    _Float16* GH    = (_Float16*)(ws + F_GH);
+
+    int nppF = 0;
+    const int cands[6] = {20000, 10000, 5000, 2500, 1250, 625};
+    for (int i = 0; i < 6; ++i)
+        if (ws_size >= NEED_F(cands[i])) { nppF = cands[i]; break; }
+    if (nppF == 0) return;
 
     detect_idx_kernel<<<1, 1, 0, stream>>>(eidx, flag);
     hipMemsetAsync(ws + OFF_HIST, 0, NN * sizeof(int), stream);
-
-    int S = 0;
-    if (ws_size >= NEED_S(20000)) S = 1;
-    else if (ws_size >= NEED_S(10000)) S = 2;
-    else if (ws_size >= NEED_S(5000))  S = 4;
-    else if (ws_size >= NEED_S(2500))  S = 8;
-
-    if (S > 0) {
-        int* outd = (int*)(ws + OFF_OUTD);
-        int* psP  = (int*)(ws + OFF_PSP);
-        int* curS = (int*)(ws + OFF_CURS);
-        int* dstP = (int*)(ws + OFF_DSTP);
-        int* peP  = (int*)(ws + OFF_PEP);
-        int* pdP  = (int*)(ws + OFF_PDP);
-        _Float16* G = (_Float16*)(ws + OFF_G);
-
-        hipMemsetAsync(ws + OFF_OUTD, 0, NN * sizeof(int), stream);
-
-        hist2_kernel<<<EE / 256, 256, 0, stream>>>(eidx, flag, hist, outd);
-        scan_kernel<<<1, 1024, 0, stream>>>(hist, rs, cur);
-        scanP_kernel<<<1, 1024, 0, stream>>>(outd, psP, curS);
-        scat_both_kernel<<<EE / 256, 256, 0, stream>>>(
-            eidx, flag, curS, cur, dstP, peP, pdP, srca, dsta, pe);
-        prep_kernel<<<(75904 + 255) / 256, 256, 0, stream>>>(
-            wss, wvv, wsv, wvs, wcross, W1, W2, W3, ws, 75904);
-
-        const int npp = (NN + S - 1) / S;
-        for (int s = 0; s < S; ++s) {
-            int lo = s * npp;
-            int hi = lo + npp; if (hi > NN) hi = NN;
-            gG_kernel<<<(hi - lo + 63) / 64, 256, 0, stream>>>(
-                feat0e, (const char*)ws, lo, hi, G);
-            msg0e_node_kernel<<<(hi - lo + 3) / 4, 256, 0, stream>>>(
-                feat1o, edge_attr, pos, b1, b2, b3, (const char*)ws, G, lo, hi, msg);
-        }
-        gather0_kernel<<<NN / 4, 256, 0, stream>>>(
-            feat0e, Wg, bg, (const char*)ws, msg, out);
-        msg1o_kernel<<<EE / 256, 256, 0, stream>>>(
-            feat0e, feat1o, edge_attr, pos, b1, b2, b3, (const char*)ws, msg);
-        gather1_kernel<<<NN / 4, 256, 0, stream>>>(
-            feat1o, (const char*)ws, msg, out);
-    } else {
-        hist_kernel<<<EE / 256, 256, 0, stream>>>(eidx, flag, hist);
-        scan_kernel<<<1, 1024, 0, stream>>>(hist, rs, cur);
-        scatter_r4_kernel<<<EE / 256, 256, 0, stream>>>(eidx, flag, cur, srca, dsta, pe);
-        prep_kernel<<<(43136 + 255) / 256, 256, 0, stream>>>(
-            wss, wvv, wsv, wvs, wcross, W1, W2, W3, ws, 43136);
-        msg0e_r4_kernel<<<EE / 256, 256, 0, stream>>>(
-            feat0e, feat1o, edge_attr, pos, b1, b2, b3, (const char*)ws, msg);
-        gather0_kernel<<<NN / 4, 256, 0, stream>>>(
-            feat0e, Wg, bg, (const char*)ws, msg, out);
-        msg1o_kernel<<<EE / 256, 256, 0, stream>>>(
-            feat0e, feat1o, edge_attr, pos, b1, b2, b3, (const char*)ws, msg);
-        gather1_kernel<<<NN / 4, 256, 0, stream>>>(
-            feat1o, (const char*)ws, msg, out);
-    }
-}
+    hipMemsetAsync(ws + F_OUTD, 0, NN * sizeof(int), stream);
+
+    hist2_kernel<<<EE / 256, 256, 0, stream>>>(eidx, flag, hist, outd);
+    scan_kernel<<<1, 1024, 0, stream>>>(hist, rs, cur);
+    scanP_kernel<<<1, 1024, 0, stream>>>(outd, psP, curS);
+    scat_src_kernel<<<EE / 256, 256, 0, stream>>>(
+        eidx, flag, curS, cur, dstP, pdP, posof);
+    prep2_kernel<<<(43136 + 255) / 256, 256, 0, stream>>>(
+        wss, wvv, wsv, wvs, wcross, W1, W2, W3, ws);
+
+    es_kernel<<<EE / 64, 256, 0, stream>>>(
+        edge_attr, b1, b2, b3, (const char*)ws, posof, esb);
+
+    const int S = (NN + nppF - 1) / nppF;
+    for (int s = 0; s < S; ++s) {
+        int lo = s * nppF;
+        int hi = lo + nppF; if (hi > NN) hi = NN;
+        gG2_kernel<<<(hi - lo + 63) / 64, 256, 0, stream>>>(
+            feat0e, (const char*)ws, lo, hi, GH, aux);
+        gH_kernel<<<(hi - lo + 63) / 64, 256, 0, stream>>>(
+            feat1o, (const char*)ws, lo, hi, GH, aux);
+        msg01_node_kernel<<<(hi - lo + 3) / 4, 256, 0, stream>>>(
+            pos, (const char*)ws, GH, esb, lo, hi, msg0F, msg1F);
+    }
+    gather0_kernel<<<NN / 4, 256, 0, stream>>>(
+        feat0e, Wg, bg, (const char*)ws, msg0F, out);
+    gather1_kernel<<<NN / 4, 256, 0, stream>>>(
+        feat1o, (const char*)ws, msg1F, out);
+}
```

After: 1.185 ms. 1.4x slower.
